# Kernel optimization log

Measured on AMD Instinct MI355X. Metric: run time of the kernel, lower is better.

Reference implementation:

```python
import jax, jax.numpy as jnp
import numpy as np

B, N, H, HEADS, L = 8, 64, 512, 8, 4
VOCAB, NBOND, CLS = 128, 8, 2
SP = H // HEADS
SCALE = float(np.sqrt(H))  # module divides by sqrt(hidden_dim), not sqrt(sp_dim)


def _ln(x):
    # fresh nn.LayerNorm each call -> gamma=1, beta=0
    m = jnp.mean(x, -1, keepdims=True)
    v = jnp.mean((x - m) ** 2, -1, keepdims=True)
    return (x - m) / jnp.sqrt(v + 1e-5)


def _split(x):  # [B,N,H] -> [B,h,N,sp]
    return x.reshape(B, N, HEADS, SP).transpose(0, 2, 1, 3)


def setup_inputs() -> dict:
    key = jax.random.key(0)
    ks = jax.random.split(key, 16)
    s = 0.05
    return {
        "input_batch": jax.random.randint(ks[0], (B, N), 0, VOCAB),
        "adj_m": jax.random.randint(ks[1], (B, N, N), 0, NBOND),
        "atom_emb": jax.random.normal(ks[2], (VOCAB, H), jnp.float32) * s,
        "bond_emb": jax.random.normal(ks[3], (NBOND, H), jnp.float32) * s,
        "Wq": jax.random.normal(ks[4], (L, H, H), jnp.float32) * s,
        "Wk": jax.random.normal(ks[5], (L, H, H), jnp.float32) * s,
        "Wv": jax.random.normal(ks[6], (L, H, H), jnp.float32) * s,
        "Wew": jax.random.normal(ks[7], (L, H, H), jnp.float32) * s,
        "Wstack": jax.random.normal(ks[8], (L, H, H), jnp.float32) * s,
        "Wf1": jax.random.normal(ks[9], (L, H, 4 * H), jnp.float32) * s,
        "Wf2": jax.random.normal(ks[10], (L, 4 * H, H), jnp.float32) * s,
        "Wout": jax.random.normal(ks[11], (H, H), jnp.float32) * s,
        "Wpred": jax.random.normal(ks[12], (H, CLS), jnp.float32) * s,
        "bpred": jnp.zeros((CLS,), jnp.float32),
    }


def _forward(input_batch, adj_m, atom_emb, bond_emb, Wq, Wk, Wv, Wew,
             Wstack, Wf1, Wf2, Wout, Wpred, bpred):
    x = atom_emb[input_batch]        # [B,N,H] atom embeddings
    bond = bond_emb[adj_m]           # [B,N,N,H] bond embeddings
    neg = jnp.where(adj_m > 0, 0.0, -jnp.inf)[:, None, :, :]  # [B,1,N,N]
    for l in range(L):
        xn = _ln(x)
        q = _split(xn @ Wq[l])
        k = _split(xn @ Wk[l])
        v = _split(xn @ Wv[l])
        ew = bond @ Wew[l]           # [B,N,N,H]
        w = ew.reshape(B, N, N, HEADS, SP).transpose(0, 3, 1, 2, 4)  # [B,h,N,N,sp]
        # bond_influence==1: sim_ij = q_i . (k_j + w_ij)
        logits = jnp.einsum('bhid,bhjd->bhij', q, k) \
               + jnp.einsum('bhid,bhijd->bhij', q, w)
        attn = jax.nn.softmax(logits / SCALE + neg, axis=-1)
        o = jnp.einsum('bhij,bhjd->bhid', attn, v)
        o = o.transpose(0, 2, 1, 3).reshape(B, N, H) @ Wstack[l]
        attn_resid = o + xn
        ff = jax.nn.relu(_ln(attn_resid) @ Wf1[l]) @ Wf2[l]
        x = ff + attn_resid          # transformer_output
        # edge attention update: softmax over {w.w, w.x_i, w.x_j}
        ew_s = jnp.sum(ew * ew, -1)                      # [B,N,N]
        a0 = jnp.einsum('bijh,bih->bij', ew, x)
        a1 = jnp.einsum('bijh,bjh->bij', ew, x)
        wgt = jax.nn.softmax(jnp.stack([ew_s, a0, a1], -1) / SCALE, -1)  # [B,N,N,3]
        bond = (wgt[..., 0:1] * ew
                + wgt[..., 1:2] * x[:, :, None, :]
                + wgt[..., 2:3] * x[:, None, :, :])      # new edge state
    cls = jnp.tanh(x[:, 0, :] @ Wout)
    return jax.nn.softmax(cls @ Wpred + bpred, axis=-1)


def reference(input_batch, adj_m, atom_emb, bond_emb, Wq, Wk, Wv, Wew,
              Wstack, Wf1, Wf2, Wout, Wpred, bpred):
    return _forward(input_batch, adj_m, atom_emb, bond_emb, Wq, Wk, Wv, Wew,
                    Wstack, Wf1, Wf2, Wout, Wpred, bpred)
```

## Files before the change

kernel.cpp:

```cpp
#include <hip/hip_runtime.h>
#include <hip/hip_bf16.h>

typedef __hip_bfloat16 bf16;

#define B_     8
#define N_     64
#define H_     512
#define HEADS_ 8
#define SP_    64
#define L_     4
static constexpr float INV_SCALE = 0.044194173824159216f;

typedef __attribute__((ext_vector_type(8))) short short8;
typedef __attribute__((ext_vector_type(4))) float f32x4;

__device__ __forceinline__ void unpack8(uint4 u, float* f) {
    f[0] = __uint_as_float(u.x << 16); f[1] = __uint_as_float(u.x & 0xffff0000u);
    f[2] = __uint_as_float(u.y << 16); f[3] = __uint_as_float(u.y & 0xffff0000u);
    f[4] = __uint_as_float(u.z << 16); f[5] = __uint_as_float(u.z & 0xffff0000u);
    f[6] = __uint_as_float(u.w << 16); f[7] = __uint_as_float(u.w & 0xffff0000u);
}

__device__ __forceinline__ bf16 f2bf(float v) { return __float2bfloat16(v); }

__device__ __forceinline__ uint4 pack8bf(float4 a, float4 b) {
    __align__(16) bf16 t[8];
    t[0] = f2bf(a.x); t[1] = f2bf(a.y); t[2] = f2bf(a.z); t[3] = f2bf(a.w);
    t[4] = f2bf(b.x); t[5] = f2bf(b.y); t[6] = f2bf(b.z); t[7] = f2bf(b.w);
    return *(const uint4*)t;
}

#define RSTR 80

template <int EPI>
__device__ __forceinline__ void gemm64_body(char* lds,
        const bf16* __restrict__ A, const bf16* __restrict__ Bt,
        void* __restrict__ Cv, const float* __restrict__ R,
        int M, int N, int K, int bx, int by, int kbeg, int kend) {
    char* As = lds;
    char* Bs = lds + 2 * 64 * RSTR;
    const int tid = threadIdx.x;
    const int bm = bx * 64, bn = by * 64;
    const int w = tid >> 6, lane = tid & 63;
    const int wr = (w >> 1) * 32, wc = (w & 1) * 32;
    const int m0 = lane & 15, q4 = lane >> 4;

    f32x4 acc[2][2] = {};

    const int rA = tid >> 3;
    const int cA = tid & 7;
    const int ksP = cA >> 2;
    const int cB = (cA & 3) * 16;
    const int cE = cA * 8;

    for (int k0 = kbeg; k0 < kend; k0 += 64) {
        uint4 a0 = *(const uint4*)(A  + (size_t)(bm + rA) * K + k0 + cE);
        uint4 a1 = *(const uint4*)(A  + (size_t)(bm + rA + 32) * K + k0 + cE);
        uint4 b0 = *(const uint4*)(Bt + (size_t)(bn + rA) * K + k0 + cE);
        uint4 b1 = *(const uint4*)(Bt + (size_t)(bn + rA + 32) * K + k0 + cE);
        __syncthreads();
        *(uint4*)(As + ksP * (64 * RSTR) + rA * RSTR + cB) = a0;
        *(uint4*)(As + ksP * (64 * RSTR) + (rA + 32) * RSTR + cB) = a1;
        *(uint4*)(Bs + ksP * (64 * RSTR) + rA * RSTR + cB) = b0;
        *(uint4*)(Bs + ksP * (64 * RSTR) + (rA + 32) * RSTR + cB) = b1;
        __syncthreads();
        short8 af[2][2], bfr[2][2];
        #pragma unroll
        for (int ks = 0; ks < 2; ++ks)
            #pragma unroll
            for (int t = 0; t < 2; ++t) {
                af[ks][t]  = *(const short8*)(As + ks * (64 * RSTR) + (wr + t * 16 + m0) * RSTR + q4 * 16);
                bfr[ks][t] = *(const short8*)(Bs + ks * (64 * RSTR) + (wc + t * 16 + m0) * RSTR + q4 * 16);
            }
        #pragma unroll
        for (int ks = 0; ks < 2; ++ks)
            #pragma unroll
            for (int mt = 0; mt < 2; ++mt)
                #pragma unroll
                for (int nt = 0; nt < 2; ++nt)
                    acc[mt][nt] = __builtin_amdgcn_mfma_f32_16x16x32_bf16(
                        af[ks][mt], bfr[ks][nt], acc[mt][nt], 0, 0, 0);
    }

    if (EPI <= 1) {
        float* C = (float*)Cv;
        #pragma unroll
        for (int mt = 0; mt < 2; ++mt)
            #pragma unroll
            for (int i = 0; i < 4; ++i) {
                int row = bm + wr + mt * 16 + q4 * 4 + i;
                #pragma unroll
                for (int nt = 0; nt < 2; ++nt) {
                    int col = bn + wc + nt * 16 + m0;
                    float v = acc[mt][nt][i];
                    if (EPI == 1) v += R[(size_t)row * N + col];
                    C[(size_t)row * N + col] = v;
                }
            }
    } else {
        bf16* C = (bf16*)Cv;
        #pragma unroll
        for (int mt = 0; mt < 2; ++mt)
            #pragma unroll
            for (int i = 0; i < 4; ++i) {
                int row = bm + wr + mt * 16 + q4 * 4 + i;
                #pragma unroll
                for (int nt = 0; nt < 2; ++nt) {
                    int col = bn + wc + nt * 16 + m0;
                    float v = acc[mt][nt][i];
                    if (EPI == 2) v = fmaxf(v, 0.0f);
                    C[(size_t)row * N + col] = __float2bfloat16(v);
                }
            }
    }
}

template <int EPI, bool SPLIT>
__launch_bounds__(256)
__global__ void mfma_gemm_s(const bf16* __restrict__ A, const bf16* __restrict__ Bt,
                            void* __restrict__ Cv, const float* __restrict__ R,
                            int M, int N, int K) {
    __shared__ __align__(16) char lds[4 * 64 * RSTR];
    int kbeg = 0, kend = K;
    const bf16* B2 = Bt;
    void* C2 = Cv;
    if (SPLIT) {
        int ks = K / gridDim.z;
        kbeg = blockIdx.z * ks;
        kend = kbeg + ks;
        C2 = (void*)((float*)Cv + (size_t)blockIdx.z * M * N);
        gemm64_body<0>(lds, A, B2, C2, nullptr, M, N, K, blockIdx.x, blockIdx.y, kbeg, kend);
    } else {
        B2 = Bt + (size_t)blockIdx.z * N * K;
        if (EPI <= 1) C2 = (void*)((float*)Cv + (size_t)blockIdx.z * M * N);
        gemm64_body<EPI>(lds, A, B2, C2, R, M, N, K, blockIdx.x, blockIdx.y, kbeg, kend);
    }
}

__launch_bounds__(256)
__global__ void basis1_qkv_kernel(const bf16* __restrict__ x_bf, const bf16* __restrict__ E0,
                                  const bf16* __restrict__ ewt1,
                                  bf16* __restrict__ xw1, bf16* __restrict__ e0w1,
                                  const bf16* __restrict__ xn_bf, const bf16* __restrict__ qkvt_l,
                                  float* __restrict__ qkv) {
    __shared__ __align__(16) char lds[4 * 64 * RSTR];
    int bx = blockIdx.x, by = blockIdx.y;
    if (bx < 8)
        gemm64_body<3>(lds, x_bf, ewt1, xw1, nullptr, 512, 512, 512, bx, by, 0, 512);
    else if (bx == 8)
        gemm64_body<3>(lds, E0, ewt1, e0w1, nullptr, 64, 512, 512, 0, by, 0, 512);
    else {
        int tq = bx - 9;
        int z = tq >> 3, mb = tq & 7;
        gemm64_body<0>(lds, xn_bf, qkvt_l + (size_t)z * 262144,
                       qkv + (size_t)z * 262144, nullptr, 512, 512, 512, mb, by, 0, 512);
    }
}

__launch_bounds__(256)
__global__ void basis2_qkv_kernel(const bf16* __restrict__ xw1, const bf16* __restrict__ x_bf,
                                  const bf16* __restrict__ e0w1, const bf16* __restrict__ ewt2,
                                  bf16* __restrict__ xw12, bf16* __restrict__ x2w2,
                                  bf16* __restrict__ e0w12,
                                  const bf16* __restrict__ xn_bf, const bf16* __restrict__ qkvt_l,
                                  float* __restrict__ qkv) {
    __shared__ __align__(16) char lds[4 * 64 * RSTR];
    int bx = blockIdx.x, by = blockIdx.y;
    if (bx < 8)
        gemm64_body<3>(lds, xw1, ewt2, xw12, nullptr, 512, 512, 512, bx, by, 0, 512);
    else if (bx < 16)
        gemm64_body<3>(lds, x_bf, ewt2, x2w2, nullptr, 512, 512, 512, bx - 8, by, 0, 512);
    else if (bx == 16)
        gemm64_body<3>(lds, e0w1, ewt2, e0w12, nullptr, 64, 512, 512, 0, by, 0, 512);
    else {
        int tq = bx - 17;
        int z = tq >> 3, mb = tq & 7;
        gemm64_body<0>(lds, xn_bf, qkvt_l + (size_t)z * 262144,
                       qkv + (size_t)z * 262144, nullptr, 512, 512, 512, mb, by, 0, 512);
    }
}

__launch_bounds__(256)
__global__ void ptable_kernel(const float* __restrict__ q,
                              const bf16* __restrict__ B0, const bf16* __restrict__ B1,
                              const bf16* __restrict__ B2,
                              float* __restrict__ P0, float* __restrict__ P1,
                              float* __restrict__ P2) {
    __shared__ __align__(16) char lds[4 * 64 * RSTR];
    char* As = lds;
    char* Bs = lds + 2 * 64 * RSTR;
    const int b = blockIdx.x, h = blockIdx.y, z = blockIdx.z;
    const int nz = gridDim.z;
    const bf16* Bt = (z == 0) ? B0 : (z == 1 ? B1 : B2);
    float* P = (z == 0) ? P0 : (z == 1 ? P1 : P2);
    const bool shr = (z == nz - 1);
    const int tid = threadIdx.x;
    const int w = tid >> 6, lane = tid & 63;
    const int wr = (w >> 1) * 32, wc = (w & 1) * 32;
    const int m0 = lane & 15, q4 = lane >> 4;
    const int rA = tid >> 3;
    const int cA = tid & 7;
    const int ksP = cA >> 2;
    const int cB = (cA & 3) * 16;
    const int cE = cA * 8;

    const float* Aq = q + (size_t)(b * 64) * 512 + h * 64;
    const bf16*  Bb = Bt + (shr ? (size_t)0 : (size_t)b * 64 * 512) + h * 64;

    float4 fa0 = *(const float4*)(Aq + (size_t)rA * 512 + cE);
    float4 fa1 = *(const float4*)(Aq + (size_t)rA * 512 + cE + 4);
    float4 fb0 = *(const float4*)(Aq + (size_t)(rA + 32) * 512 + cE);
    float4 fb1 = *(const float4*)(Aq + (size_t)(rA + 32) * 512 + cE + 4);
    uint4 bv0 = *(const uint4*)(Bb + (size_t)rA * 512 + cE);
    uint4 bv1 = *(const uint4*)(Bb + (size_t)(rA + 32) * 512 + cE);
    uint4 av0 = pack8bf(fa0, fa1);
    uint4 av1 = pack8bf(fb0, fb1);
    *(uint4*)(As + ksP * (64 * RSTR) + rA * RSTR + cB) = av0;
    *(uint4*)(As + ksP * (64 * RSTR) + (rA + 32) * RSTR + cB) = av1;
    *(uint4*)(Bs + ksP * (64 * RSTR) + rA * RSTR + cB) = bv0;
    *(uint4*)(Bs + ksP * (64 * RSTR) + (rA + 32) * RSTR + cB) = bv1;
    __syncthreads();

    f32x4 acc[2][2] = {};
    short8 af[2][2], bfr[2][2];
    #pragma unroll
    for (int ks = 0; ks < 2; ++ks)
        #pragma unroll
        for (int t = 0; t < 2; ++t) {
            af[ks][t]  = *(const short8*)(As + ks * (64 * RSTR) + (wr + t * 16 + m0) * RSTR + q4 * 16);
            bfr[ks][t] = *(const short8*)(Bs + ks * (64 * RSTR) + (wc + t * 16 + m0) * RSTR + q4 * 16);
        }
    #pragma unroll
    for (int ks = 0; ks < 2; ++ks)
        #pragma unroll
        for (int mt = 0; mt < 2; ++mt)
            #pragma unroll
            for (int nt = 0; nt < 2; ++nt)
                acc[mt][nt] = __builtin_amdgcn_mfma_f32_16x16x32_bf16(
                    af[ks][mt], bfr[ks][nt], acc[mt][nt], 0, 0, 0);

    #pragma unroll
    for (int mt = 0; mt < 2; ++mt)
        #pragma unroll
        for (int i = 0; i < 4; ++i) {
            int row = wr + mt * 16 + q4 * 4 + i;
            #pragma unroll
            for (int nt = 0; nt < 2; ++nt) {
                int col = wc + nt * 16 + m0;
                P[(((size_t)b * 8 + h) * 64 + row) * 64 + col] = acc[mt][nt][i];
            }
        }
}

__launch_bounds__(256)
__global__ void gram1_kernel(const bf16* __restrict__ xw1, const bf16* __restrict__ e0w1,
                             const bf16* __restrict__ xb, float* __restrict__ gbuf) {
    __shared__ __align__(16) char lds[4 * 64 * RSTR];
    int b = blockIdx.x, z = blockIdx.y;
    size_t ob = (size_t)b * 32768;
    const bf16 *A, *Bt;
    switch (z) {
        case 0: A = xw1 + ob; Bt = xw1 + ob; break;
        case 1: A = e0w1;     Bt = xw1 + ob; break;
        case 2: A = xw1 + ob; Bt = xb + ob;  break;
        case 3: A = e0w1;     Bt = xb + ob;  break;
        default: A = e0w1;    Bt = e0w1;     break;
    }
    float* C = gbuf + (size_t)z * 32768 + (size_t)b * 4096;
    gemm64_body<0>(lds, A, Bt, C, nullptr, 64, 64, 512, 0, 0, 0, 512);
}

__launch_bounds__(256)
__global__ void gram2_kernel(const bf16* __restrict__ xw12, const bf16* __restrict__ x2w2,
                             const bf16* __restrict__ e0w12, const bf16* __restrict__ xb,
                             float* __restrict__ gbuf) {
    __shared__ __align__(16) char lds[4 * 64 * RSTR];
    int b = blockIdx.x, z = blockIdx.y;
    size_t ob = (size_t)b * 32768;
    const bf16 *A, *Bt;
    switch (z) {
        case 0: A = xw12 + ob; Bt = xw12 + ob; break;
        case 1: A = xw12 + ob; Bt = x2w2 + ob; break;
        case 2: A = x2w2 + ob; Bt = x2w2 + ob; break;
        case 3: A = e0w12;     Bt = xw12 + ob; break;
        case 4: A = e0w12;     Bt = x2w2 + ob; break;
        case 5: A = e0w12;     Bt = e0w12;     break;
        case 6: A = xw12 + ob; Bt = xb + ob;   break;
        case 7: A = x2w2 + ob; Bt = xb + ob;   break;
        default: A = e0w12;    Bt = xb + ob;   break;
    }
    float* C = gbuf + (size_t)z * 32768 + (size_t)b * 4096;
    gemm64_body<0>(lds, A, Bt, C, nullptr, 64, 64, 512, 0, 0, 0, 512);
}

__global__ void coeff_assemble1(const int* __restrict__ adj,
        const float* __restrict__ c0a, const float* __restrict__ c1a, const float* __restrict__ c2a,
        const float* __restrict__ gbuf,
        float* __restrict__ w0o, float* __restrict__ w1o, float* __restrict__ w2o) {
    int bi = blockIdx.x;
    int b = bi >> 6, i = bi & 63;
    int j = threadIdx.x;
    int p = bi * 64 + j;
    int t = adj[p];
    const float* TXX = gbuf + 0 * 32768 + (size_t)b * 4096;
    const float* TEX = gbuf + 1 * 32768 + (size_t)b * 4096;
    const float* TXx = gbuf + 2 * 32768 + (size_t)b * 4096;
    const float* TEx = gbuf + 3 * 32768 + (size_t)b * 4096;
    const float* TEE = gbuf + 4 * 32768 + (size_t)b * 4096;
    float c0 = c0a[p], c1 = c1a[p], c2 = c2a[p];
    float s1 = c0 * TEx[t * 64 + i] + c1 * TXx[i * 64 + i] + c2 * TXx[j * 64 + i];
    float s2 = c0 * TEx[t * 64 + j] + c1 * TXx[i * 64 + j] + c2 * TXx[j * 64 + j];
    float s0 = c0 * c0 * TEE[t * 64 + t] + c1 * c1 * TXX[i * 64 + i] + c2 * c2 * TXX[j * 64 + j]
             + 2.f * c0 * c1 * TEX[t * 64 + i] + 2.f * c0 * c2 * TEX[t * 64 + j]
             + 2.f * c1 * c2 * TXX[i * 64 + j];
    float t0 = s0 * INV_SCALE, t1 = s1 * INV_SCALE, t2 = s2 * INV_SCALE;
    float m = fmaxf(t0, fmaxf(t1, t2));
    float e0 = expf(t0 - m), e1 = expf(t1 - m), e2 = expf(t2 - m);
    float inv = 1.0f / (e0 + e1 + e2);
    w0o[p] = e0 * inv;
    w1o[p] = e1 * inv;
    w2o[p] = e2 * inv;
}

__global__ void coeff_assemble2(const int* __restrict__ adj,
        const float* __restrict__ c0a, const float* __restrict__ c1a, const float* __restrict__ c2a,
        const float* __restrict__ c0b, const float* __restrict__ c1b, const float* __restrict__ c2b,
        const float* __restrict__ gbuf,
        float* __restrict__ w0o, float* __restrict__ w1o, float* __restrict__ w2o) {
    int bi = blockIdx.x;
    int b = bi >> 6, i = bi & 63;
    int j = threadIdx.x;
    int p = bi * 64 + j;
    int t = adj[p];
    const float* TXX = gbuf + 0 * 32768 + (size_t)b * 4096;
    const float* TXY = gbuf + 1 * 32768 + (size_t)b * 4096;
    const float* TYY = gbuf + 2 * 32768 + (size_t)b * 4096;
    const float* TEX = gbuf + 3 * 32768 + (size_t)b * 4096;
    const float* TEY = gbuf + 4 * 32768 + (size_t)b * 4096;
    const float* TEE = gbuf + 5 * 32768 + (size_t)b * 4096;
    const float* TXx = gbuf + 6 * 32768 + (size_t)b * 4096;
    const float* TYx = gbuf + 7 * 32768 + (size_t)b * 4096;
    const float* TEx = gbuf + 8 * 32768 + (size_t)b * 4096;
    float a0 = c0b[p];
    float AE = a0 * c0a[p], Aa = a0 * c1a[p], Ab = a0 * c2a[p];
    float Ac = c1b[p], Ad = c2b[p];
    float s1 = AE * TEx[t * 64 + i] + Aa * TXx[i * 64 + i] + Ab * TXx[j * 64 + i]
             + Ac * TYx[i * 64 + i] + Ad * TYx[j * 64 + i];
    float s2 = AE * TEx[t * 64 + j] + Aa * TXx[i * 64 + j] + Ab * TXx[j * 64 + j]
             + Ac * TYx[i * 64 + j] + Ad * TYx[j * 64 + j];
    float s0 = AE * AE * TEE[t * 64 + t] + Aa * Aa * TXX[i * 64 + i] + Ab * Ab * TXX[j * 64 + j]
             + Ac * Ac * TYY[i * 64 + i] + Ad * Ad * TYY[j * 64 + j]
             + 2.f * AE * Aa * TEX[t * 64 + i] + 2.f * AE * Ab * TEX[t * 64 + j]
             + 2.f * AE * Ac * TEY[t * 64 + i] + 2.f * AE * Ad * TEY[t * 64 + j]
             + 2.f * Aa * Ab * TXX[i * 64 + j]
             + 2.f * Aa * Ac * TXY[i * 64 + i] + 2.f * Aa * Ad * TXY[i * 64 + j]
             + 2.f * Ab * Ac * TXY[j * 64 + i] + 2.f * Ab * Ad * TXY[j * 64 + j]
             + 2.f * Ac * Ad * TYY[i * 64 + j];
    float t0 = s0 * INV_SCALE, t1 = s1 * INV_SCALE, t2 = s2 * INV_SCALE;
    float m = fmaxf(t0, fmaxf(t1, t2));
    float e0 = expf(t0 - m), e1 = expf(t1 - m), e2 = expf(t2 - m);
    float inv = 1.0f / (e0 + e1 + e2);
    w0o[p] = e0 * inv;
    w1o[p] = e1 * inv;
    w2o[p] = e2 * inv;
}

__launch_bounds__(256)
__global__ void u_gemm(const float* __restrict__ q, const bf16* __restrict__ wc3,
                       bf16* __restrict__ ubf) {
    __shared__ __align__(16) char lds[4 * 64 * RSTR];
    char* As = lds;
    char* Bs = lds + 2 * 64 * RSTR;
    const int h = blockIdx.x, mb = blockIdx.y, nb = blockIdx.z;
    const int tid = threadIdx.x;
    const int w = tid >> 6, lane = tid & 63;
    const int wr = (w >> 1) * 32, wc = (w & 1) * 32;
    const int m0 = lane & 15, q4 = lane >> 4;
    const int rA = tid >> 3;
    const int cA = tid & 7;
    const int ksP = cA >> 2;
    const int cB = (cA & 3) * 16;
    const int cE = cA * 8;

    const float* Aq = q + (size_t)(mb * 64) * 512 + h * 64;
    const bf16*  Bt = wc3 + (size_t)(nb * 64) * 512 + h * 64;

    float4 fa0 = *(const float4*)(Aq + (size_t)rA * 512 + cE);
    float4 fa1 = *(const float4*)(Aq + (size_t)rA * 512 + cE + 4);
    float4 fb0 = *(const float4*)(Aq + (size_t)(rA + 32) * 512 + cE);
    float4 fb1 = *(const float4*)(Aq + (size_t)(rA + 32) * 512 + cE + 4);
    uint4 b0 = *(const uint4*)(Bt + (size_t)rA * 512 + cE);
    uint4 b1 = *(const uint4*)(Bt + (size_t)(rA + 32) * 512 + cE);
    uint4 a0 = pack8bf(fa0, fa1);
    uint4 a1 = pack8bf(fb0, fb1);
    *(uint4*)(As + ksP * (64 * RSTR) + rA * RSTR + cB) = a0;
    *(uint4*)(As + ksP * (64 * RSTR) + (rA + 32) * RSTR + cB) = a1;
    *(uint4*)(Bs + ksP * (64 * RSTR) + rA * RSTR + cB) = b0;
    *(uint4*)(Bs + ksP * (64 * RSTR) + (rA + 32) * RSTR + cB) = b1;
    __syncthreads();

    f32x4 acc[2][2] = {};
    short8 af[2][2], bfr[2][2];
    #pragma unroll
    for (int ks = 0; ks < 2; ++ks)
        #pragma unroll
        for (int t = 0; t < 2; ++t) {
            af[ks][t]  = *(const short8*)(As + ks * (64 * RSTR) + (wr + t * 16 + m0) * RSTR + q4 * 16);
            bfr[ks][t] = *(const short8*)(Bs + ks * (64 * RSTR) + (wc + t * 16 + m0) * RSTR + q4 * 16);
        }
    #pragma unroll
    for (int ks = 0; ks < 2; ++ks)
        #pragma unroll
        for (int mt = 0; mt < 2; ++mt)
            #pragma unroll
            for (int nt = 0; nt < 2; ++nt)
                acc[mt][nt] = __builtin_amdgcn_mfma_f32_16x16x32_bf16(
                    af[ks][mt], bfr[ks][nt], acc[mt][nt], 0, 0, 0);

    #pragma unroll
    for (int mt = 0; mt < 2; ++mt)
        #pragma unroll
        for (int i = 0; i < 4; ++i) {
            int row = mb * 64 + wr + mt * 16 + q4 * 4 + i;
            #pragma unroll
            for (int nt = 0; nt < 2; ++nt) {
                int col = nb * 64 + wc + nt * 16 + m0;
                ubf[(size_t)row * 4096 + h * 512 + col] = f2bf(acc[mt][nt][i]);
            }
        }
}

__global__ void cast_w3(const float* __restrict__ in, bf16* __restrict__ out) {
    int gid = blockIdx.x * 256 + threadIdx.x;
    const float4* p = (const float4*)(in + (size_t)gid * 8);
    float4 a = p[0], b = p[1];
    *(uint4*)(out + (size_t)gid * 8) = pack8bf(a, b);
}

__launch_bounds__(256)
__global__ void mbuf_gemm(const bf16* __restrict__ ubf, const bf16* __restrict__ xw12,
                          const bf16* __restrict__ x2w2, const bf16* __restrict__ x_bf,
                          const bf16* __restrict__ e0w12,
                          float* __restrict__ MX, float* __restrict__ MY,
                          float* __restrict__ MZ, float* __restrict__ DE) {
    __shared__ __align__(16) char lds[4 * 64 * RSTR];
    int b = blockIdx.x, mt = blockIdx.y, z = blockIdx.z;
    const bf16* A = ubf + (size_t)b * 512 * 512;
    const bf16* Bt;
    float* C;
    if (z == 0)      { Bt = xw12 + (size_t)b * 64 * 512; C = MX + (size_t)b * 512 * 64; }
    else if (z == 1) { Bt = x2w2 + (size_t)b * 64 * 512; C = MY + (size_t)b * 512 * 64; }
    else if (z == 2) { Bt = x_bf + (size_t)b * 64 * 512; C = MZ + (size_t)b * 512 * 64; }
    else             { Bt = e0w12;                        C = DE + (size_t)b * 512 * 64; }
    gemm64_body<0>(lds, A, Bt, C, nullptr, 512, 64, 512, mt, 0, 0, 512);
}

__global__ void s2_assemble(const int* __restrict__ adj,
        const float* __restrict__ c0a, const float* __restrict__ c1a, const float* __restrict__ c2a,
        const float* __restrict__ c0b, const float* __restrict__ c1b, const float* __restrict__ c2b,
        const float* __restrict__ v0c, const float* __restrict__ v1c, const float* __restrict__ v2c,
        const float* __restrict__ MX, const float* __restrict__ MY,
        const float* __restrict__ MZ, const float* __restrict__ DE,
        float* __restrict__ s2) {
    int bi = blockIdx.x;
    int b = bi >> 6, i = bi & 63;
    int j = threadIdx.x, h = threadIdx.y;
    int p = bi * 64 + j;
    float v0 = v0c[p];
    float q0 = v0 * c0b[p];
    float AE = q0 * c0a[p], Aa = q0 * c1a[p], Ab = q0 * c2a[p];
    float Ac = v0 * c1b[p], Ad = v0 * c2b[p];
    float Ae = v1c[p], Af = v2c[p];
    size_t rb = ((size_t)b * 512 + i * 8 + h) * 64;
    float s = AE * DE[rb + adj[p]]
            + Aa * MX[rb + i] + Ac * MY[rb + i] + Ae * MZ[rb + i]
            + Ab * MX[rb + j] + Ad * MY[rb + j] + Af * MZ[rb + j];
    s2[(((size_t)b * 8 + h) * 64 + i) * 64 + j] = s;
}

__global__ void embed_ln_kernel(const int* __restrict__ ids,
                                const float* __restrict__ emb,
                                float* __restrict__ xn, bf16* __restrict__ xn_bf) {
    int row = blockIdx.x;
    int tid = threadIdx.x;
    const float* r = emb + (size_t)ids[row] * H_;
    float x0 = r[tid], x1 = r[tid + 256];
    float s = x0 + x1, sq = x0 * x0 + x1 * x1;
    #pragma unroll
    for (int off = 32; off; off >>= 1) {
        s  += __shfl_xor(s,  off);
        sq += __shfl_xor(sq, off);
    }
    __shared__ float ls[4], lq[4];
    int w = tid >> 6;
    if ((tid & 63) == 0) { ls[w] = s; lq[w] = sq; }
    __syncthreads();
    float S = ls[0] + ls[1] + ls[2] + ls[3];
    float Q = lq[0] + lq[1] + lq[2] + lq[3];
    float mean = S * (1.0f / H_);
    float var  = Q * (1.0f / H_) - mean * mean;
    float inv  = rsqrtf(var + 1e-5f);
    float y0 = (x0 - mean) * inv, y1 = (x1 - mean) * inv;
    xn[(size_t)row * H_ + tid]       = y0;
    xn[(size_t)row * H_ + tid + 256] = y1;
    xn_bf[(size_t)row * H_ + tid]       = f2bf(y0);
    xn_bf[(size_t)row * H_ + tid + 256] = f2bf(y1);
}

__global__ void ew0_precompute(const float* __restrict__ bond_emb,
                               const bf16* __restrict__ ewt0, bf16* __restrict__ E0) {
    int t = blockIdx.x, cb = blockIdx.y, lane = threadIdx.x;
    int c = cb * 64 + lane;
    if (t >= 8) { E0[t * 512 + c] = f2bf(0.0f); return; }
    __shared__ float be[512];
    for (int h = lane; h < 512; h += 64) be[h] = bond_emb[t * 512 + h];
    __syncthreads();
    const bf16* wr = ewt0 + (size_t)c * 512;
    float acc = 0.f;
    for (int h8 = 0; h8 < 64; ++h8) {
        uint4 u = *(const uint4*)(wr + h8 * 8);
        float wf[8];
        unpack8(u, wf);
        const float* b = &be[h8 * 8];
        acc += b[0]*wf[0] + b[1]*wf[1] + b[2]*wf[2] + b[3]*wf[3]
             + b[4]*wf[4] + b[5]*wf[5] + b[6]*wf[6] + b[7]*wf[7];
    }
    E0[t * 512 + c] = f2bf(acc);
}

__global__ void transpose_sq(const float* __restrict__ Wq, const float* __restrict__ Wk,
                             const float* __restrict__ Wv, const float* __restrict__ Wew,
                             const float* __restrict__ Wst,
                             bf16* __restrict__ qkvt, bf16* __restrict__ ewt,
                             bf16* __restrict__ stackt) {
    const size_t KN = (size_t)H_ * H_;
    int z = blockIdx.z;
    const float* W; bf16* Wt;
    if (z < 12) {
        int s = z >> 2, l = z & 3;
        W  = (s == 0 ? Wq : s == 1 ? Wk : Wv) + (size_t)l * KN;
        Wt = qkvt + (size_t)l * 3 * KN + (size_t)s * KN;
    } else if (z < 16) {
        int l = z - 12;
        W = Wew + (size_t)l * KN; Wt = ewt + (size_t)l * KN;
    } else {
        int l = z - 16;
        W = Wst + (size_t)l * KN; Wt = stackt + (size_t)l * KN;
    }
    __shared__ float t[32][33];
    int k0 = blockIdx.x * 32, n0 = blockIdx.y * 32;
    int tx = threadIdx.x, ty = threadIdx.y;
    #pragma unroll
    for (int r = ty; r < 32; r += 8)
        t[r][tx] = W[(size_t)(k0 + r) * H_ + n0 + tx];
    __syncthreads();
    #pragma unroll
    for (int r = ty; r < 32; r += 8)
        Wt[(size_t)(n0 + r) * H_ + k0 + tx] = f2bf(t[tx][r]);
}

__global__ void transpose_rect(const float* __restrict__ Wf1, const float* __restrict__ Wf2,
                               bf16* __restrict__ f1t, bf16* __restrict__ f2t) {
    const size_t KN4 = (size_t)4 * H_ * H_;
    int z = blockIdx.z;
    const float* W; bf16* Wt; int K, N;
    if (z < 4) {
        if (blockIdx.x >= 16) return;
        W = Wf1 + (size_t)z * KN4; Wt = f1t + (size_t)z * KN4; K = 512; N = 2048;
    } else {
        if (blockIdx.y >= 16) return;
        W = Wf2 + (size_t)(z - 4) * KN4; Wt = f2t + (size_t)(z - 4) * KN4; K = 2048; N = 512;
    }
    __shared__ float t[32][33];
    int k0 = blockIdx.x * 32, n0 = blockIdx.y * 32;
    int tx = threadIdx.x, ty = threadIdx.y;
    #pragma unroll
    for (int r = ty; r < 32; r += 8)
        t[r][tx] = W[(size_t)(k0 + r) * N + n0 + tx];
    __syncthreads();
    #pragma unroll
    for (int r = ty; r < 32; r += 8)
        Wt[(size_t)(n0 + r) * K + k0 + tx] = f2bf(t[tx][r]);
}

__global__ void reduce_stack_ln(const float* __restrict__ part, const float* __restrict__ base,
                                float* __restrict__ resid, bf16* __restrict__ ffin_bf) {
    const int MN = 512 * H_;
    int row = blockIdx.x;
    int tid = threadIdx.x;
    size_t b0 = (size_t)row * H_;
    float v0 = base[b0 + tid], v1 = base[b0 + tid + 256];
    #pragma unroll
    for (int s = 0; s < 4; ++s) {
        v0 += part[(size_t)s * MN + b0 + tid];
        v1 += part[(size_t)s * MN + b0 + tid + 256];
    }
    resid[b0 + tid] = v0;
    resid[b0 + tid + 256] = v1;
    float s = v0 + v1, sq = v0 * v0 + v1 * v1;
    #pragma unroll
    for (int off = 32; off; off >>= 1) {
        s  += __shfl_xor(s,  off);
        sq += __shfl_xor(sq, off);
    }
    __shared__ float ls[4], lq[4];
    int w = tid >> 6;
    if ((tid & 63) == 0) { ls[w] = s; lq[w] = sq; }
    __syncthreads();
    float S = ls[0] + ls[1] + ls[2] + ls[3];
    float Q = lq[0] + lq[1] + lq[2] + lq[3];
    float mean = S * (1.0f / H_);
    float var  = Q * (1.0f / H_) - mean * mean;
    float inv  = rsqrtf(var + 1e-5f);
    ffin_bf[b0 + tid]       = f2bf((v0 - mean) * inv);
    ffin_bf[b0 + tid + 256] = f2bf((v1 - mean) * inv);
}

template <bool DO_LN>
__global__ void reduce_ln_kernel(const float* __restrict__ part, const float* __restrict__ resid,
                                 float* __restrict__ x, bf16* __restrict__ x_bf,
                                 float* __restrict__ xn, bf16* __restrict__ xn_bf) {
    const int MN = 512 * H_;
    int row = blockIdx.x;
    int tid = threadIdx.x;
    size_t base = (size_t)row * H_;
    float v0 = resid[base + tid], v1 = resid[base + tid + 256];
    #pragma unroll
    for (int s = 0; s < 4; ++s) {
        v0 += part[(size_t)s * MN + base + tid];
        v1 += part[(size_t)s * MN + base + tid + 256];
    }
    x[base + tid] = v0;
    x[base + tid + 256] = v1;
    x_bf[base + tid]       = f2bf(v0);
    x_bf[base + tid + 256] = f2bf(v1);
    if (DO_LN) {
        float s = v0 + v1, sq = v0 * v0 + v1 * v1;
        #pragma unroll
        for (int off = 32; off; off >>= 1) {
            s  += __shfl_xor(s,  off);
            sq += __shfl_xor(sq, off);
        }
        __shared__ float ls[4], lq[4];
        int w = tid >> 6;
        if ((tid & 63) == 0) { ls[w] = s; lq[w] = sq; }
        __syncthreads();
        float S = ls[0] + ls[1] + ls[2] + ls[3];
        float Q = lq[0] + lq[1] + lq[2] + lq[3];
        float mean = S * (1.0f / H_);
        float var  = Q * (1.0f / H_) - mean * mean;
        float inv  = rsqrtf(var + 1e-5f);
        float y0 = (v0 - mean) * inv, y1 = (v1 - mean) * inv;
        xn[base + tid]       = y0;
        xn[base + tid + 256] = y1;
        xn_bf[base + tid]       = f2bf(y0);
        xn_bf[base + tid + 256] = f2bf(y1);
    }
}

template <bool GATHER>
__global__ void attn_kernel(const float* __restrict__ qkv, const bf16* __restrict__ ew,
                            const int* __restrict__ adj, bf16* __restrict__ o) {
    const float* q = qkv;
    const float* k = qkv + (size_t)512 * H_;
    const float* v = qkv + (size_t)1024 * H_;
    int bi = blockIdx.x;
    int b  = bi >> 6;
    int ty = threadIdx.y;
    int h  = blockIdx.y * 4 + ty;
    int lane = threadIdx.x;
    __shared__ float qs[4][64], as[4][64];
    qs[ty][lane] = q[(size_t)bi * H_ + h * 64 + lane];
    __syncthreads();

    int j = lane;
    int pair = bi * 64 + j;
    int aj = adj[pair];
    const float4* k4 = (const float4*)(k + (size_t)(b * 64 + j) * H_ + h * 64);
    const uint4*  w4 = (const uint4*)((GATHER ? ew + (size_t)aj * H_
                                              : ew + (size_t)pair * H_) + h * 64);
    float acc = 0.f;
    #pragma unroll
    for (int t = 0; t < 8; ++t) {
        uint4 wu = w4[t];
        float4 ka = k4[2 * t], kb = k4[2 * t + 1];
        float wf[8];
        unpack8(wu, wf);
        const float* qq = &qs[ty][t * 8];
        acc += qq[0] * (ka.x + wf[0]) + qq[1] * (ka.y + wf[1])
             + qq[2] * (ka.z + wf[2]) + qq[3] * (ka.w + wf[3])
             + qq[4] * (kb.x + wf[4]) + qq[5] * (kb.y + wf[5])
             + qq[6] * (kb.z + wf[6]) + qq[7] * (kb.w + wf[7]);
    }
    float logit = acc * INV_SCALE;
    if (aj <= 0) logit = -INFINITY;

    float m = logit;
    #pragma unroll
    for (int off = 32; off; off >>= 1) m = fmaxf(m, __shfl_xor(m, off));
    float p = expf(logit - m);
    float s = p;
    #pragma unroll
    for (int off = 32; off; off >>= 1) s += __shfl_xor(s, off);
    as[ty][lane] = p / s;
    __syncthreads();

    const float* vbase = v + (size_t)(b * 64) * H_ + h * 64;
    float oacc = 0.f;
    int d = lane;
    #pragma unroll 8
    for (int jj = 0; jj < 64; ++jj)
        oacc += as[ty][jj] * vbase[(size_t)jj * H_ + d];
    o[(size_t)bi * H_ + h * 64 + d] = __float2bfloat16(oacc);
}

template <int MODE>
__global__ void attn13_kernel(const float* __restrict__ qkv, const int* __restrict__ adj,
        const float* __restrict__ c0a, const float* __restrict__ c1a, const float* __restrict__ c2a,
        const float* __restrict__ c0b, const float* __restrict__ c1b, const float* __restrict__ c2b,
        const float* __restrict__ PX, const float* __restrict__ PY, const float* __restrict__ PE,
        bf16* __restrict__ o) {
    const float* q = qkv;
    const float* k = qkv + (size_t)512 * H_;
    const float* v = qkv + (size_t)1024 * H_;
    int bi = blockIdx.x;
    int b  = bi >> 6, i = bi & 63;
    int ty = threadIdx.y;
    int h  = blockIdx.y * 4 + ty;
    int lane = threadIdx.x;
    __shared__ float qs[4][64], as[4][64];
    qs[ty][lane] = q[(size_t)bi * H_ + h * 64 + lane];
    __syncthreads();

    int j = lane;
    int p = bi * 64 + j;
    int t = adj[p];
    size_t pb = (((size_t)b * 8 + h) * 64 + i) * 64;
    float acc;
    if (MODE == 1) {
        acc = c0a[p] * PE[pb + t] + c1a[p] * PX[pb + i] + c2a[p] * PX[pb + j];
    } else {
        float a0 = c0b[p];
        float AE = a0 * c0a[p], Aa = a0 * c1a[p], Ab = a0 * c2a[p];
        float Ac = c1b[p], Ad = c2b[p];
        acc = AE * PE[pb + t] + Aa * PX[pb + i] + Ab * PX[pb + j]
            + Ac * PY[pb + i] + Ad * PY[pb + j];
    }
    const float4* k4 = (const float4*)(k + (size_t)(b * 64 + j) * H_ + h * 64);
    #pragma unroll
    for (int tt = 0; tt < 8; ++tt) {
        float4 ka = k4[2 * tt], kb = k4[2 * tt + 1];
        const float* qq = &qs[ty][tt * 8];
        acc += qq[0] * ka.x + qq[1] * ka.y + qq[2] * ka.z + qq[3] * ka.w
             + qq[4] * kb.x + qq[5] * kb.y + qq[6] * kb.z + qq[7] * kb.w;
    }
    float logit = acc * INV_SCALE;
    if (t <= 0) logit = -INFINITY;

    float m = logit;
    #pragma unroll
    for (int off = 32; off; off >>= 1) m = fmaxf(m, __shfl_xor(m, off));
    float pe = expf(logit - m);
    float s = pe;
    #pragma unroll
    for (int off = 32; off; off >>= 1) s += __shfl_xor(s, off);
    as[ty][lane] = pe / s;
    __syncthreads();

    const float* vbase = v + (size_t)(b * 64) * H_ + h * 64;
    float oacc = 0.f;
    int d = lane;
    #pragma unroll 8
    for (int jj = 0; jj < 64; ++jj)
        oacc += as[ty][jj] * vbase[(size_t)jj * H_ + d];
    o[(size_t)bi * H_ + h * 64 + d] = __float2bfloat16(oacc);
}

__global__ void attn3_kernel(const float* __restrict__ qkv, const float* __restrict__ s2,
                             const int* __restrict__ adj, bf16* __restrict__ o) {
    const float* q = qkv;
    const float* k = qkv + (size_t)512 * H_;
    const float* v = qkv + (size_t)1024 * H_;
    int bi = blockIdx.x;
    int b  = bi >> 6, i = bi & 63;
    int ty = threadIdx.y;
    int h  = blockIdx.y * 4 + ty;
    int lane = threadIdx.x;
    __shared__ float qs[4][64], as[4][64];
    qs[ty][lane] = q[(size_t)bi * H_ + h * 64 + lane];
    __syncthreads();

    int j = lane;
    const float4* k4 = (const float4*)(k + (size_t)(b * 64 + j) * H_ + h * 64);
    float acc = s2[(((size_t)b * 8 + h) * 64 + i) * 64 + j];
    #pragma unroll
    for (int t = 0; t < 8; ++t) {
        float4 ka = k4[2 * t], kb = k4[2 * t + 1];
        const float* qq = &qs[ty][t * 8];
        acc += qq[0] * ka.x + qq[1] * ka.y + qq[2] * ka.z + qq[3] * ka.w
             + qq[4] * kb.x + qq[5] * kb.y + qq[6] * kb.z + qq[7] * kb.w;
    }
    float logit = acc * INV_SCALE;
    if (adj[(size_t)bi * 64 + j] <= 0) logit = -INFINITY;

    float m = logit;
    #pragma unroll
    for (int off = 32; off; off >>= 1) m = fmaxf(m, __shfl_xor(m, off));
    float p = expf(logit - m);
    float s = p;
    #pragma unroll
    for (int off = 32; off; off >>= 1) s += __shfl_xor(s, off);
    as[ty][lane] = p / s;
    __syncthreads();

    const float* vbase = v + (size_t)(b * 64) * H_ + h * 64;
    float oacc = 0.f;
    int d = lane;
    #pragma unroll 8
    for (int jj = 0; jj < 64; ++jj)
        oacc += as[ty][jj] * vbase[(size_t)jj * H_ + d];
    o[(size_t)bi * H_ + h * 64 + d] = __float2bfloat16(oacc);
}

template <bool GATHER>
__global__ void edge_coeff_kernel(const bf16* __restrict__ ewsrc, const int* __restrict__ adj,
                                  const float* __restrict__ x,
                                  float* __restrict__ w0o, float* __restrict__ w1o,
                                  float* __restrict__ w2o) {
    int pair = blockIdx.x * 4 + threadIdx.y;
    int b = pair >> 12;
    int i = (pair >> 6) & 63;
    int j = pair & 63;
    int lane = threadIdx.x;
    const uint4*  e4  = (const uint4*)(GATHER ? ewsrc + (size_t)adj[pair] * H_
                                              : ewsrc + (size_t)pair * H_);
    const float4* xi4 = (const float4*)(x + (size_t)(b * 64 + i) * H_);
    const float4* xj4 = (const float4*)(x + (size_t)(b * 64 + j) * H_);
    uint4  eu = e4[lane];
    float4 a0 = xi4[lane * 2], a1 = xi4[lane * 2 + 1];
    float4 c0 = xj4[lane * 2], c1 = xj4[lane * 2 + 1];
    float ef[8], af[8], cf[8];
    unpack8(eu, ef);
    af[0] = a0.x; af[1] = a0.y; af[2] = a0.z; af[3] = a0.w;
    af[4] = a1.x; af[5] = a1.y; af[6] = a1.z; af[7] = a1.w;
    cf[0] = c0.x; cf[1] = c0.y; cf[2] = c0.z; cf[3] = c0.w;
    cf[4] = c1.x; cf[5] = c1.y; cf[6] = c1.z; cf[7] = c1.w;
    float s0 = 0.f, s1 = 0.f, s2 = 0.f;
    #pragma unroll
    for (int t = 0; t < 8; ++t) {
        s0 += ef[t] * ef[t]; s1 += ef[t] * af[t]; s2 += ef[t] * cf[t];
    }
    #pragma unroll
    for (int off = 32; off; off >>= 1) {
        s0 += __shfl_xor(s0, off);
        s1 += __shfl_xor(s1, off);
        s2 += __shfl_xor(s2, off);
    }
    float t0 = s0 * INV_SCALE, t1 = s1 * INV_SCALE, t2 = s2 * INV_SCALE;
    float m = fmaxf(t0, fmaxf(t1, t2));
    float e0 = expf(t0 - m), e1 = expf(t1 - m), e2 = expf(t2 - m);
    float inv = 1.0f / (e0 + e1 + e2);
    if (lane == 0) {
        w0o[pair] = e0 * inv;
        w1o[pair] = e1 * inv;
        w2o[pair] = e2 * inv;
    }
}

__global__ void cls_part_kernel(const float* __restrict__ x, const float* __restrict__ Wout,
                                float* __restrict__ clspart) {
    int b  = blockIdx.x;
    int cb = blockIdx.y;
    int ks = blockIdx.z;
    int tid = threadIdx.x;
    int c  = cb * 64 + (tid & 63);
    int kk = tid >> 6;
    const float* xr = x + (size_t)(b * 64) * H_;
    int h0 = ks * 128 + kk * 32;
    float acc = 0.f;
    #pragma unroll
    for (int h = 0; h < 32; ++h)
        acc += xr[h0 + h] * Wout[(size_t)(h0 + h) * H_ + c];
    __shared__ float red[4][64];
    red[kk][tid & 63] = acc;
    __syncthreads();
    if (tid < 64) {
        float v = red[0][tid] + red[1][tid] + red[2][tid] + red[3][tid];
        clspart[((size_t)ks * 8 + b) * H_ + cb * 64 + tid] = v;
    }
}

__global__ void cls_pred2_kernel(const float* __restrict__ clspart,
                                 const float* __restrict__ Wpred,
                                 const float* __restrict__ bpred,
                                 float* __restrict__ out) {
    int b = blockIdx.x;
    int tid = threadIdx.x;
    __shared__ float red0[4], red1[4];
    float a0 = 0.f, a1 = 0.f;
    #pragma unroll
    for (int t = 0; t < 2; ++t) {
        int c = tid + t * 256;
        float v = clspart[((size_t)0 * 8 + b) * H_ + c]
                + clspart[((size_t)1 * 8 + b) * H_ + c]
                + clspart[((size_t)2 * 8 + b) * H_ + c]
                + clspart[((size_t)3 * 8 + b) * H_ + c];
        float tv = tanhf(v);
        a0 += tv * Wpred[c * 2 + 0];
        a1 += tv * Wpred[c * 2 + 1];
    }
    #pragma unroll
    for (int off = 32; off; off >>= 1) {
        a0 += __shfl_xor(a0, off);
        a1 += __shfl_xor(a1, off);
    }
    int w = tid >> 6;
    if ((tid & 63) == 0) { red0[w] = a0; red1[w] = a1; }
    __syncthreads();
    if (tid == 0) {
        float s0 = red0[0] + red0[1] + red0[2] + red0[3] + bpred[0];
        float s1 = red1[0] + red1[1] + red1[2] + red1[3] + bpred[1];
        float m = fmaxf(s0, s1);
        float e0 = expf(s0 - m), e1 = expf(s1 - m);
        float inv = 1.0f / (e0 + e1);
        out[b * 2 + 0] = e0 * inv;
        out[b * 2 + 1] = e1 * inv;
    }
}

extern "C" void kernel_launch(void* const* d_in, const int* in_sizes, int n_in,
                              void* d_out, int out_size, void* d_ws, size_t ws_size,
                              hipStream_t stream) {
    const int*   ids      = (const int*)d_in[0];
    const int*   adj      = (const int*)d_in[1];
    const float* atom_emb = (const float*)d_in[2];
    const float* bond_emb = (const float*)d_in[3];
    const float* Wq     = (const float*)d_in[4];
    const float* Wk     = (const float*)d_in[5];
    const float* Wv     = (const float*)d_in[6];
    const float* Wew    = (const float*)d_in[7];
    const float* Wstack = (const float*)d_in[8];
    const float* Wf1    = (const float*)d_in[9];
    const float* Wf2    = (const float*)d_in[10];
    const float* Wout   = (const float*)d_in[11];
    const float* Wpred  = (const float*)d_in[12];
    const float* bpred  = (const float*)d_in[13];

    char* ws = (char*)d_ws;
    size_t off = 0;
    auto alloc = [&](size_t bytes) {
        size_t o = off;
        off += (bytes + 255) & ~(size_t)255;
        return o;
    };
    const size_t ROWS  = (size_t)B_ * N_;
    const size_t PAIRS = (size_t)B_ * N_ * N_;
    const size_t KN    = (size_t)H_ * H_;

    float* x       = (float*)(ws + alloc(ROWS * H_ * 4));
    float* xn      = (float*)(ws + alloc(ROWS * H_ * 4));
    bf16*  xn_bf   = (bf16*) (ws + alloc(ROWS * H_ * 2));
    bf16*  x_bf    = (bf16*) (ws + alloc(ROWS * H_ * 2));
    float* qkv     = (float*)(ws + alloc(3 * ROWS * H_ * 4));
    bf16*  o_bf    = (bf16*) (ws + alloc(ROWS * H_ * 2));
    float* resid   = (float*)(ws + alloc(ROWS * H_ * 4));
    bf16*  ffin_bf = (bf16*) (ws + alloc(ROWS * H_ * 2));
    bf16*  ffh_bf  = (bf16*) (ws + alloc(ROWS * 4 * H_ * 2));
    float* part    = (float*)(ws + alloc(4 * ROWS * H_ * 4));
    float* clspart = (float*)(ws + alloc(4 * 8 * H_ * 4));
    bf16*  ubf     = (bf16*) (ws + alloc(ROWS * 8 * 512 * 2));
    float* s2buf   = (float*)(ws + alloc((size_t)B_ * 8 * 64 * 64 * 4));
    float* MX      = (float*)(ws + alloc((size_t)4096 * 64 * 4));
    float* MY      = (float*)(ws + alloc((size_t)4096 * 64 * 4));
    float* MZ      = (float*)(ws + alloc((size_t)4096 * 64 * 4));
    float* DE      = (float*)(ws + alloc((size_t)4096 * 64 * 4));
    float* PT0     = (float*)(ws + alloc((size_t)4096 * 64 * 4));
    float* PT1     = (float*)(ws + alloc((size_t)4096 * 64 * 4));
    float* PT2     = (float*)(ws + alloc((size_t)4096 * 64 * 4));
    float* gbuf    = (float*)(ws + alloc((size_t)9 * 8 * 4096 * 4));
    bf16*  wc3     = (bf16*) (ws + alloc(KN * 2));
    bf16*  E0      = (bf16*) (ws + alloc(64 * H_ * 2));
    bf16*  e0w1    = (bf16*) (ws + alloc(64 * H_ * 2));
    bf16*  e0w12   = (bf16*) (ws + alloc(64 * H_ * 2));
    bf16*  xw1     = (bf16*) (ws + alloc(KN * 2));
    bf16*  xw12    = (bf16*) (ws + alloc(KN * 2));
    bf16*  x2w2    = (bf16*) (ws + alloc(KN * 2));
    float* cw      = (float*)(ws + alloc(9 * PAIRS * 4));
    bf16*  qkvt    = (bf16*) (ws + alloc((size_t)L_ * 3 * KN * 2));
    bf16*  ewt     = (bf16*) (ws + alloc((size_t)L_ * KN * 2));
    bf16*  stackt  = (bf16*) (ws + alloc((size_t)L_ * KN * 2));
    bf16*  f1t     = (bf16*) (ws + alloc((size_t)L_ * 4 * KN * 2));
    bf16*  f2t     = (bf16*) (ws + alloc((size_t)L_ * 4 * KN * 2));
    (void)ws_size;

    float* cw0a = cw;
    float* cw1a = cw + PAIRS;
    float* cw2a = cw + 2 * PAIRS;
    float* cw0b = cw + 3 * PAIRS;
    float* cw1b = cw + 4 * PAIRS;
    float* cw2b = cw + 5 * PAIRS;
    float* cw0c = cw + 6 * PAIRS;
    float* cw1c = cw + 7 * PAIRS;
    float* cw2c = cw + 8 * PAIRS;

    embed_ln_kernel<<<512, 256, 0, stream>>>(ids, atom_emb, xn, xn_bf);

    dim3 tb(32, 8);
    transpose_sq<<<dim3(16, 16, 20), tb, 0, stream>>>(Wq, Wk, Wv, Wew, Wstack,
                                                      qkvt, ewt, stackt);
    transpose_rect<<<dim3(64, 64, 8), tb, 0, stream>>>(Wf1, Wf2, f1t, f2t);

    ew0_precompute<<<dim3(64, 8), 64, 0, stream>>>(bond_emb, ewt, E0);
    cast_w3<<<128, 256, 0, stream>>>(Wew + 3 * KN, wc3);

    for (int l = 0; l < L_; ++l) {
        if (l == 0) {
            mfma_gemm_s<0, false><<<dim3(8, 8, 3), 256, 0, stream>>>(
                xn_bf, qkvt, qkv, nullptr, 512, 512, 512);
            attn_kernel<true><<<dim3(512, 2), dim3(64, 4), 0, stream>>>(qkv, E0, adj, o_bf);
        } else if (l == 1) {
            basis1_qkv_kernel<<<dim3(33, 8), 256, 0, stream>>>(
                x_bf, E0, ewt + KN, xw1, e0w1, xn_bf, qkvt + (size_t)3 * KN, qkv);
            ptable_kernel<<<dim3(8, 8, 2), 256, 0, stream>>>(
                qkv, xw1, e0w1, nullptr, PT0, PT1, nullptr);
            attn13_kernel<1><<<dim3(512, 2), dim3(64, 4), 0, stream>>>(
                qkv, adj, cw0a, cw1a, cw2a, nullptr, nullptr, nullptr,
                PT0, nullptr, PT1, o_bf);
        } else if (l == 2) {
            basis2_qkv_kernel<<<dim3(41, 8), 256, 0, stream>>>(
                xw1, x_bf, e0w1, ewt + 2 * KN, xw12, x2w2, e0w12,
                xn_bf, qkvt + (size_t)6 * KN, qkv);
            ptable_kernel<<<dim3(8, 8, 3), 256, 0, stream>>>(
                qkv, xw12, x2w2, e0w12, PT0, PT1, PT2);
            attn13_kernel<2><<<dim3(512, 2), dim3(64, 4), 0, stream>>>(
                qkv, adj, cw0a, cw1a, cw2a, cw0b, cw1b, cw2b,
                PT0, PT1, PT2, o_bf);
        } else {
            mfma_gemm_s<0, false><<<dim3(8, 8, 3), 256, 0, stream>>>(
                xn_bf, qkvt + (size_t)9 * KN, qkv, nullptr, 512, 512, 512);
            u_gemm<<<dim3(8, 8, 8), 256, 0, stream>>>(qkv, wc3, ubf);
            mbuf_gemm<<<dim3(8, 8, 4), 256, 0, stream>>>(ubf, xw12, x2w2, x_bf, e0w12,
                                                         MX, MY, MZ, DE);
            s2_assemble<<<512, dim3(64, 8), 0, stream>>>(adj,
                cw0a, cw1a, cw2a, cw0b, cw1b, cw2b, cw0c, cw1c, cw2c,
                MX, MY, MZ, DE, s2buf);
            attn3_kernel<<<dim3(512, 2), dim3(64, 4), 0, stream>>>(qkv, s2buf, adj, o_bf);
        }

        mfma_gemm_s<0, true><<<dim3(8, 8, 4), 256, 0, stream>>>(
            o_bf, stackt + (size_t)l * KN, part, nullptr, 512, 512, 512);
        reduce_stack_ln<<<512, 256, 0, stream>>>(part, xn, resid, ffin_bf);
        mfma_gemm_s<2, false><<<dim3(8, 32), 256, 0, stream>>>(
            ffin_bf, f1t + (size_t)l * 4 * KN, ffh_bf, nullptr, 512, 2048, 512);
        mfma_gemm_s<0, true><<<dim3(8, 8, 4), 256, 0, stream>>>(
            ffh_bf, f2t + (size_t)l * 4 * KN, part, nullptr, 512, 512, 2048);
        if (l < L_ - 1)
            reduce_ln_kernel<true><<<512, 256, 0, stream>>>(part, resid, x, x_bf, xn, xn_bf);
        else
            reduce_ln_kernel<false><<<512, 256, 0, stream>>>(part, resid, x, x_bf, xn, xn_bf);

        if (l == 0) {
            edge_coeff_kernel<true><<<8192, dim3(64, 4), 0, stream>>>(
                E0, adj, x, cw0a, cw1a, cw2a);
        } else if (l == 1) {
            gram1_kernel<<<dim3(8, 5), 256, 0, stream>>>(xw1, e0w1, x_bf, gbuf);
            coeff_assemble1<<<512, 64, 0, stream>>>(adj, cw0a, cw1a, cw2a, gbuf,
                                                    cw0b, cw1b, cw2b);
        } else if (l == 2) {
            gram2_kernel<<<dim3(8, 9), 256, 0, stream>>>(xw12, x2w2, e0w12, x_bf, gbuf);
            coeff_assemble2<<<512, 64, 0, stream>>>(adj, cw0a, cw1a, cw2a,
                                                    cw0b, cw1b, cw2b, gbuf,
                                                    cw0c, cw1c, cw2c);
        }
    }

    cls_part_kernel<<<dim3(8, 8, 4), 256, 0, stream>>>(x, Wout, clspart);
    cls_pred2_kernel<<<8, 256, 0, stream>>>(clspart, Wpred, bpred, (float*)d_out);
}
```

Baseline: 393.5 us.

## Fuse setup, edge-coefficient, gram and assembly kernels into fewer launches

Merges the five setup kernels (embed+LN, weight transposes, E0 precompute, W3 cast) into one large setup kernel. It also folds each layer's edge-coefficient, gram and coefficient-assembly work into the next layer's basis/QKV, ptable and u-gemm kernels. The s2 assembly is fused into the layer-3 attention kernel, which removes the s2buf round trip. The aim is to cut kernel-launch count and small-grid latency across the dependency chain, at the cost of heterogeneous, branchy blocks and tighter cross-stage ordering.

```diff
diff --git a/kernel.cpp b/kernel.cpp
--- a/kernel.cpp
+++ b/kernel.cpp
@@ -137,63 +137,11 @@
     }
 }
 
-__launch_bounds__(256)
-__global__ void basis1_qkv_kernel(const bf16* __restrict__ x_bf, const bf16* __restrict__ E0,
-                                  const bf16* __restrict__ ewt1,
-                                  bf16* __restrict__ xw1, bf16* __restrict__ e0w1,
-                                  const bf16* __restrict__ xn_bf, const bf16* __restrict__ qkvt_l,
-                                  float* __restrict__ qkv) {
-    __shared__ __align__(16) char lds[4 * 64 * RSTR];
-    int bx = blockIdx.x, by = blockIdx.y;
-    if (bx < 8)
-        gemm64_body<3>(lds, x_bf, ewt1, xw1, nullptr, 512, 512, 512, bx, by, 0, 512);
-    else if (bx == 8)
-        gemm64_body<3>(lds, E0, ewt1, e0w1, nullptr, 64, 512, 512, 0, by, 0, 512);
-    else {
-        int tq = bx - 9;
-        int z = tq >> 3, mb = tq & 7;
-        gemm64_body<0>(lds, xn_bf, qkvt_l + (size_t)z * 262144,
-                       qkv + (size_t)z * 262144, nullptr, 512, 512, 512, mb, by, 0, 512);
-    }
-}
-
-__launch_bounds__(256)
-__global__ void basis2_qkv_kernel(const bf16* __restrict__ xw1, const bf16* __restrict__ x_bf,
-                                  const bf16* __restrict__ e0w1, const bf16* __restrict__ ewt2,
-                                  bf16* __restrict__ xw12, bf16* __restrict__ x2w2,
-                                  bf16* __restrict__ e0w12,
-                                  const bf16* __restrict__ xn_bf, const bf16* __restrict__ qkvt_l,
-                                  float* __restrict__ qkv) {
-    __shared__ __align__(16) char lds[4 * 64 * RSTR];
-    int bx = blockIdx.x, by = blockIdx.y;
-    if (bx < 8)
-        gemm64_body<3>(lds, xw1, ewt2, xw12, nullptr, 512, 512, 512, bx, by, 0, 512);
-    else if (bx < 16)
-        gemm64_body<3>(lds, x_bf, ewt2, x2w2, nullptr, 512, 512, 512, bx - 8, by, 0, 512);
-    else if (bx == 16)
-        gemm64_body<3>(lds, e0w1, ewt2, e0w12, nullptr, 64, 512, 512, 0, by, 0, 512);
-    else {
-        int tq = bx - 17;
-        int z = tq >> 3, mb = tq & 7;
-        gemm64_body<0>(lds, xn_bf, qkvt_l + (size_t)z * 262144,
-                       qkv + (size_t)z * 262144, nullptr, 512, 512, 512, mb, by, 0, 512);
-    }
-}
-
-__launch_bounds__(256)
-__global__ void ptable_kernel(const float* __restrict__ q,
-                              const bf16* __restrict__ B0, const bf16* __restrict__ B1,
-                              const bf16* __restrict__ B2,
-                              float* __restrict__ P0, float* __restrict__ P1,
-                              float* __restrict__ P2) {
-    __shared__ __align__(16) char lds[4 * 64 * RSTR];
+
+__device__ __forceinline__ void ptable_body(char* lds, const float* __restrict__ q,
+        const bf16* __restrict__ Bt, float* __restrict__ P, int b, int h, bool shr) {
     char* As = lds;
     char* Bs = lds + 2 * 64 * RSTR;
-    const int b = blockIdx.x, h = blockIdx.y, z = blockIdx.z;
-    const int nz = gridDim.z;
-    const bf16* Bt = (z == 0) ? B0 : (z == 1 ? B1 : B2);
-    float* P = (z == 0) ? P0 : (z == 1 ? P1 : P2);
-    const bool shr = (z == nz - 1);
     const int tid = threadIdx.x;
     const int w = tid >> 6, lane = tid & 63;
     const int wr = (w >> 1) * 32, wc = (w & 1) * 32;
@@ -252,55 +200,74 @@
         }
 }
 
-__launch_bounds__(256)
-__global__ void gram1_kernel(const bf16* __restrict__ xw1, const bf16* __restrict__ e0w1,
-                             const bf16* __restrict__ xb, float* __restrict__ gbuf) {
-    __shared__ __align__(16) char lds[4 * 64 * RSTR];
-    int b = blockIdx.x, z = blockIdx.y;
-    size_t ob = (size_t)b * 32768;
-    const bf16 *A, *Bt;
-    switch (z) {
-        case 0: A = xw1 + ob; Bt = xw1 + ob; break;
-        case 1: A = e0w1;     Bt = xw1 + ob; break;
-        case 2: A = xw1 + ob; Bt = xb + ob;  break;
-        case 3: A = e0w1;     Bt = xb + ob;  break;
-        default: A = e0w1;    Bt = e0w1;     break;
-    }
-    float* C = gbuf + (size_t)z * 32768 + (size_t)b * 4096;
-    gemm64_body<0>(lds, A, Bt, C, nullptr, 64, 64, 512, 0, 0, 0, 512);
-}
-
-__launch_bounds__(256)
-__global__ void gram2_kernel(const bf16* __restrict__ xw12, const bf16* __restrict__ x2w2,
-                             const bf16* __restrict__ e0w12, const bf16* __restrict__ xb,
-                             float* __restrict__ gbuf) {
-    __shared__ __align__(16) char lds[4 * 64 * RSTR];
-    int b = blockIdx.x, z = blockIdx.y;
-    size_t ob = (size_t)b * 32768;
-    const bf16 *A, *Bt;
-    switch (z) {
-        case 0: A = xw12 + ob; Bt = xw12 + ob; break;
-        case 1: A = xw12 + ob; Bt = x2w2 + ob; break;
-        case 2: A = x2w2 + ob; Bt = x2w2 + ob; break;
-        case 3: A = e0w12;     Bt = xw12 + ob; break;
-        case 4: A = e0w12;     Bt = x2w2 + ob; break;
-        case 5: A = e0w12;     Bt = e0w12;     break;
-        case 6: A = xw12 + ob; Bt = xb + ob;   break;
-        case 7: A = x2w2 + ob; Bt = xb + ob;   break;
-        default: A = e0w12;    Bt = xb + ob;   break;
-    }
-    float* C = gbuf + (size_t)z * 32768 + (size_t)b * 4096;
-    gemm64_body<0>(lds, A, Bt, C, nullptr, 64, 64, 512, 0, 0, 0, 512);
-}
-
-__global__ void coeff_assemble1(const int* __restrict__ adj,
+__device__ __forceinline__ void ugemm_body(char* lds, const float* __restrict__ q,
+        const bf16* __restrict__ wc3, bf16* __restrict__ ubf, int h, int mb, int nb) {
+    char* As = lds;
+    char* Bs = lds + 2 * 64 * RSTR;
+    const int tid = threadIdx.x;
+    const int w = tid >> 6, lane = tid & 63;
+    const int wr = (w >> 1) * 32, wc = (w & 1) * 32;
+    const int m0 = lane & 15, q4 = lane >> 4;
+    const int rA = tid >> 3;
+    const int cA = tid & 7;
+    const int ksP = cA >> 2;
+    const int cB = (cA & 3) * 16;
+    const int cE = cA * 8;
+
+    const float* Aq = q + (size_t)(mb * 64) * 512 + h * 64;
+    const bf16*  Bt = wc3 + (size_t)(nb * 64) * 512 + h * 64;
+
+    float4 fa0 = *(const float4*)(Aq + (size_t)rA * 512 + cE);
+    float4 fa1 = *(const float4*)(Aq + (size_t)rA * 512 + cE + 4);
+    float4 fb0 = *(const float4*)(Aq + (size_t)(rA + 32) * 512 + cE);
+    float4 fb1 = *(const float4*)(Aq + (size_t)(rA + 32) * 512 + cE + 4);
+    uint4 b0 = *(const uint4*)(Bt + (size_t)rA * 512 + cE);
+    uint4 b1 = *(const uint4*)(Bt + (size_t)(rA + 32) * 512 + cE);
+    uint4 a0 = pack8bf(fa0, fa1);
+    uint4 a1 = pack8bf(fb0, fb1);
+    *(uint4*)(As + ksP * (64 * RSTR) + rA * RSTR + cB) = a0;
+    *(uint4*)(As + ksP * (64 * RSTR) + (rA + 32) * RSTR + cB) = a1;
+    *(uint4*)(Bs + ksP * (64 * RSTR) + rA * RSTR + cB) = b0;
+    *(uint4*)(Bs + ksP * (64 * RSTR) + (rA + 32) * RSTR + cB) = b1;
+    __syncthreads();
+
+    f32x4 acc[2][2] = {};
+    short8 af[2][2], bfr[2][2];
+    #pragma unroll
+    for (int ks = 0; ks < 2; ++ks)
+        #pragma unroll
+        for (int t = 0; t < 2; ++t) {
+            af[ks][t]  = *(const short8*)(As + ks * (64 * RSTR) + (wr + t * 16 + m0) * RSTR + q4 * 16);
+            bfr[ks][t] = *(const short8*)(Bs + ks * (64 * RSTR) + (wc + t * 16 + m0) * RSTR + q4 * 16);
+        }
+    #pragma unroll
+    for (int ks = 0; ks < 2; ++ks)
+        #pragma unroll
+        for (int mt = 0; mt < 2; ++mt)
+            #pragma unroll
+            for (int nt = 0; nt < 2; ++nt)
+                acc[mt][nt] = __builtin_amdgcn_mfma_f32_16x16x32_bf16(
+                    af[ks][mt], bfr[ks][nt], acc[mt][nt], 0, 0, 0);
+
+    #pragma unroll
+    for (int mt = 0; mt < 2; ++mt)
+        #pragma unroll
+        for (int i = 0; i < 4; ++i) {
+            int row = mb * 64 + wr + mt * 16 + q4 * 4 + i;
+            #pragma unroll
+            for (int nt = 0; nt < 2; ++nt) {
+                int col = nb * 64 + wc + nt * 16 + m0;
+                ubf[(size_t)row * 4096 + h * 512 + col] = f2bf(acc[mt][nt][i]);
+            }
+        }
+}
+
+__device__ __forceinline__ void coeff1_body(const int* __restrict__ adj,
         const float* __restrict__ c0a, const float* __restrict__ c1a, const float* __restrict__ c2a,
-        const float* __restrict__ gbuf,
+        const float* __restrict__ gbuf, int row, int j,
         float* __restrict__ w0o, float* __restrict__ w1o, float* __restrict__ w2o) {
-    int bi = blockIdx.x;
-    int b = bi >> 6, i = bi & 63;
-    int j = threadIdx.x;
-    int p = bi * 64 + j;
+    int b = row >> 6, i = row & 63;
+    int p = row * 64 + j;
     int t = adj[p];
     const float* TXX = gbuf + 0 * 32768 + (size_t)b * 4096;
     const float* TEX = gbuf + 1 * 32768 + (size_t)b * 4096;
@@ -322,15 +289,13 @@
     w2o[p] = e2 * inv;
 }
 
-__global__ void coeff_assemble2(const int* __restrict__ adj,
+__device__ __forceinline__ void coeff2_body(const int* __restrict__ adj,
         const float* __restrict__ c0a, const float* __restrict__ c1a, const float* __restrict__ c2a,
         const float* __restrict__ c0b, const float* __restrict__ c1b, const float* __restrict__ c2b,
-        const float* __restrict__ gbuf,
+        const float* __restrict__ gbuf, int row, int j,
         float* __restrict__ w0o, float* __restrict__ w1o, float* __restrict__ w2o) {
-    int bi = blockIdx.x;
-    int b = bi >> 6, i = bi & 63;
-    int j = threadIdx.x;
-    int p = bi * 64 + j;
+    int b = row >> 6, i = row & 63;
+    int p = row * 64 + j;
     int t = adj[p];
     const float* TXX = gbuf + 0 * 32768 + (size_t)b * 4096;
     const float* TXY = gbuf + 1 * 32768 + (size_t)b * 4096;
@@ -366,75 +331,328 @@
 }
 
 __launch_bounds__(256)
-__global__ void u_gemm(const float* __restrict__ q, const bf16* __restrict__ wc3,
-                       bf16* __restrict__ ubf) {
+__global__ void setup_kernel(const int* __restrict__ ids, const float* __restrict__ atom_emb,
+                             const float* __restrict__ bond_emb,
+                             const float* __restrict__ Wq, const float* __restrict__ Wk,
+                             const float* __restrict__ Wv, const float* __restrict__ Wew,
+                             const float* __restrict__ Wst,
+                             const float* __restrict__ Wf1, const float* __restrict__ Wf2,
+                             float* __restrict__ xn, bf16* __restrict__ xn_bf,
+                             bf16* __restrict__ qkvt, bf16* __restrict__ ewt,
+                             bf16* __restrict__ stackt,
+                             bf16* __restrict__ f1t, bf16* __restrict__ f2t,
+                             bf16* __restrict__ E0, bf16* __restrict__ wc3) {
+    __shared__ float smem[32 * 33 + 8];
+    const size_t KN = (size_t)H_ * H_;
+    int bid = blockIdx.x;
+    int tid = threadIdx.x;
+
+    if (bid < 512) {
+        int row = bid;
+        const float* r = atom_emb + (size_t)ids[row] * H_;
+        float x0 = r[tid], x1 = r[tid + 256];
+        float s = x0 + x1, sq = x0 * x0 + x1 * x1;
+        #pragma unroll
+        for (int off = 32; off; off >>= 1) {
+            s  += __shfl_xor(s,  off);
+            sq += __shfl_xor(sq, off);
+        }
+        int w = tid >> 6;
+        if ((tid & 63) == 0) { smem[w] = s; smem[4 + w] = sq; }
+        __syncthreads();
+        float S = smem[0] + smem[1] + smem[2] + smem[3];
+        float Q = smem[4] + smem[5] + smem[6] + smem[7];
+        float mean = S * (1.0f / H_);
+        float var  = Q * (1.0f / H_) - mean * mean;
+        float inv  = rsqrtf(var + 1e-5f);
+        float y0 = (x0 - mean) * inv, y1 = (x1 - mean) * inv;
+        xn[(size_t)row * H_ + tid]       = y0;
+        xn[(size_t)row * H_ + tid + 256] = y1;
+        xn_bf[(size_t)row * H_ + tid]       = f2bf(y0);
+        xn_bf[(size_t)row * H_ + tid + 256] = f2bf(y1);
+    } else if (bid < 5632) {
+        int idx = bid - 512;
+        int z = idx >> 8;
+        int rem = idx & 255;
+        int byv = rem >> 4, bxv = rem & 15;
+        const float* W; bf16* Wt;
+        if (z < 12) {
+            int sss = z >> 2, l = z & 3;
+            W  = (sss == 0 ? Wq : sss == 1 ? Wk : Wv) + (size_t)l * KN;
+            Wt = qkvt + (size_t)l * 3 * KN + (size_t)sss * KN;
+        } else if (z < 16) {
+            int l = z - 12;
+            W = Wew + (size_t)l * KN; Wt = ewt + (size_t)l * KN;
+        } else {
+            int l = z - 16;
+            W = Wst + (size_t)l * KN; Wt = stackt + (size_t)l * KN;
+        }
+        float (*tt)[33] = (float(*)[33])smem;
+        int k0 = bxv * 32, n0 = byv * 32;
+        int tx = tid & 31, tyv = tid >> 5;
+        #pragma unroll
+        for (int rr = tyv; rr < 32; rr += 8)
+            tt[rr][tx] = W[(size_t)(k0 + rr) * H_ + n0 + tx];
+        __syncthreads();
+        #pragma unroll
+        for (int rr = tyv; rr < 32; rr += 8)
+            Wt[(size_t)(n0 + rr) * H_ + k0 + tx] = f2bf(tt[tx][rr]);
+    } else if (bid < 13824) {
+        int idx = bid - 5632;
+        int z = idx >> 10;
+        int idx2 = idx & 1023;
+        const size_t KN4 = (size_t)4 * H_ * H_;
+        const float* W; bf16* Wt; int K, N, kb, nb;
+        if (z < 4) {
+            W = Wf1 + (size_t)z * KN4; Wt = f1t + (size_t)z * KN4; K = 512; N = 2048;
+            kb = idx2 & 15; nb = idx2 >> 4;
+        } else {
+            W = Wf2 + (size_t)(z - 4) * KN4; Wt = f2t + (size_t)(z - 4) * KN4; K = 2048; N = 512;
+            kb = idx2 & 63; nb = idx2 >> 6;
+        }
+        float (*tt)[33] = (float(*)[33])smem;
+        int k0 = kb * 32, n0 = nb * 32;
+        int tx = tid & 31, tyv = tid >> 5;
+        #pragma unroll
+        for (int rr = tyv; rr < 32; rr += 8)
+            tt[rr][tx] = W[(size_t)(k0 + rr) * N + n0 + tx];
+        __syncthreads();
+        #pragma unroll
+        for (int rr = tyv; rr < 32; rr += 8)
+            Wt[(size_t)(n0 + rr) * K + k0 + tx] = f2bf(tt[tx][rr]);
+    } else if (bid < 13952) {
+        int idx = bid - 13824;
+        int t = idx >> 1;
+        int c = (idx & 1) * 256 + tid;
+        if (t >= 8) { E0[t * 512 + c] = f2bf(0.0f); return; }
+        float* be = smem;
+        be[tid]       = bond_emb[t * 512 + tid];
+        be[tid + 256] = bond_emb[t * 512 + tid + 256];
+        __syncthreads();
+        float acc = 0.f;
+        #pragma unroll 8
+        for (int h = 0; h < 512; ++h)
+            acc += be[h] * Wew[(size_t)h * 512 + c];
+        E0[t * 512 + c] = f2bf(acc);
+    } else {
+        int idx = bid - 13952;
+        int gid = idx * 256 + tid;
+        const float4* p = (const float4*)(Wew + 3 * KN + (size_t)gid * 8);
+        float4 a = p[0], b = p[1];
+        *(uint4*)(wc3 + (size_t)gid * 8) = pack8bf(a, b);
+    }
+}
+
+__launch_bounds__(256)
+__global__ void basis1_qkv_ec(const bf16* __restrict__ x_bf, const bf16* __restrict__ E0,
+                              const bf16* __restrict__ ewt1,
+                              bf16* __restrict__ xw1, bf16* __restrict__ e0w1,
+                              const bf16* __restrict__ xn_bf, const bf16* __restrict__ qkvt_l,
+                              float* __restrict__ qkv,
+                              const int* __restrict__ adj, const float* __restrict__ x,
+                              float* __restrict__ w0o, float* __restrict__ w1o,
+                              float* __restrict__ w2o) {
     __shared__ __align__(16) char lds[4 * 64 * RSTR];
-    char* As = lds;
-    char* Bs = lds + 2 * 64 * RSTR;
-    const int h = blockIdx.x, mb = blockIdx.y, nb = blockIdx.z;
-    const int tid = threadIdx.x;
-    const int w = tid >> 6, lane = tid & 63;
-    const int wr = (w >> 1) * 32, wc = (w & 1) * 32;
-    const int m0 = lane & 15, q4 = lane >> 4;
-    const int rA = tid >> 3;
-    const int cA = tid & 7;
-    const int ksP = cA >> 2;
-    const int cB = (cA & 3) * 16;
-    const int cE = cA * 8;
-
-    const float* Aq = q + (size_t)(mb * 64) * 512 + h * 64;
-    const bf16*  Bt = wc3 + (size_t)(nb * 64) * 512 + h * 64;
-
-    float4 fa0 = *(const float4*)(Aq + (size_t)rA * 512 + cE);
-    float4 fa1 = *(const float4*)(Aq + (size_t)rA * 512 + cE + 4);
-    float4 fb0 = *(const float4*)(Aq + (size_t)(rA + 32) * 512 + cE);
-    float4 fb1 = *(const float4*)(Aq + (size_t)(rA + 32) * 512 + cE + 4);
-    uint4 b0 = *(const uint4*)(Bt + (size_t)rA * 512 + cE);
-    uint4 b1 = *(const uint4*)(Bt + (size_t)(rA + 32) * 512 + cE);
-    uint4 a0 = pack8bf(fa0, fa1);
-    uint4 a1 = pack8bf(fb0, fb1);
-    *(uint4*)(As + ksP * (64 * RSTR) + rA * RSTR + cB) = a0;
-    *(uint4*)(As + ksP * (64 * RSTR) + (rA + 32) * RSTR + cB) = a1;
-    *(uint4*)(Bs + ksP * (64 * RSTR) + rA * RSTR + cB) = b0;
-    *(uint4*)(Bs + ksP * (64 * RSTR) + (rA + 32) * RSTR + cB) = b1;
-    __syncthreads();
-
-    f32x4 acc[2][2] = {};
-    short8 af[2][2], bfr[2][2];
-    #pragma unroll
-    for (int ks = 0; ks < 2; ++ks)
-        #pragma unroll
-        for (int t = 0; t < 2; ++t) {
-            af[ks][t]  = *(const short8*)(As + ks * (64 * RSTR) + (wr + t * 16 + m0) * RSTR + q4 * 16);
-            bfr[ks][t] = *(const short8*)(Bs + ks * (64 * RSTR) + (wc + t * 16 + m0) * RSTR + q4 * 16);
-        }
-    #pragma unroll
-    for (int ks = 0; ks < 2; ++ks)
-        #pragma unroll
-        for (int mt = 0; mt < 2; ++mt)
+    int bid = blockIdx.x;
+    if (bid < 264) {
+        int bx = bid >> 3, by = bid & 7;
+        if (bx < 8)
+            gemm64_body<3>(lds, x_bf, ewt1, xw1, nullptr, 512, 512, 512, bx, by, 0, 512);
+        else if (bx == 8)
+            gemm64_body<3>(lds, E0, ewt1, e0w1, nullptr, 64, 512, 512, 0, by, 0, 512);
+        else {
+            int tq = bx - 9;
+            int z = tq >> 3, mb = tq & 7;
+            gemm64_body<0>(lds, xn_bf, qkvt_l + (size_t)z * 262144,
+                           qkv + (size_t)z * 262144, nullptr, 512, 512, 512, mb, by, 0, 512);
+        }
+    } else {
+        int k = bid - 264;
+        int tid = threadIdx.x;
+        int lane = tid & 63, tyv = tid >> 6;
+        for (int pp = 0; pp < 4; ++pp) {
+            int pair = k * 16 + pp * 4 + tyv;
+            int b = pair >> 12;
+            int i = (pair >> 6) & 63;
+            int j = pair & 63;
+            const uint4*  e4  = (const uint4*)(E0 + (size_t)adj[pair] * H_);
+            const float4* xi4 = (const float4*)(x + (size_t)(b * 64 + i) * H_);
+            const float4* xj4 = (const float4*)(x + (size_t)(b * 64 + j) * H_);
+            uint4  eu = e4[lane];
+            float4 a0 = xi4[lane * 2], a1 = xi4[lane * 2 + 1];
+            float4 c0 = xj4[lane * 2], c1 = xj4[lane * 2 + 1];
+            float ef[8], af[8], cf[8];
+            unpack8(eu, ef);
+            af[0] = a0.x; af[1] = a0.y; af[2] = a0.z; af[3] = a0.w;
+            af[4] = a1.x; af[5] = a1.y; af[6] = a1.z; af[7] = a1.w;
+            cf[0] = c0.x; cf[1] = c0.y; cf[2] = c0.z; cf[3] = c0.w;
+            cf[4] = c1.x; cf[5] = c1.y; cf[6] = c1.z; cf[7] = c1.w;
+            float s0 = 0.f, s1 = 0.f, s2 = 0.f;
             #pragma unroll
-            for (int nt = 0; nt < 2; ++nt)
-                acc[mt][nt] = __builtin_amdgcn_mfma_f32_16x16x32_bf16(
-                    af[ks][mt], bfr[ks][nt], acc[mt][nt], 0, 0, 0);
-
-    #pragma unroll
-    for (int mt = 0; mt < 2; ++mt)
-        #pragma unroll
-        for (int i = 0; i < 4; ++i) {
-            int row = mb * 64 + wr + mt * 16 + q4 * 4 + i;
+            for (int t = 0; t < 8; ++t) {
+                s0 += ef[t] * ef[t]; s1 += ef[t] * af[t]; s2 += ef[t] * cf[t];
+            }
             #pragma unroll
-            for (int nt = 0; nt < 2; ++nt) {
-                int col = nb * 64 + wc + nt * 16 + m0;
-                ubf[(size_t)row * 4096 + h * 512 + col] = f2bf(acc[mt][nt][i]);
+            for (int off = 32; off; off >>= 1) {
+                s0 += __shfl_xor(s0, off);
+                s1 += __shfl_xor(s1, off);
+                s2 += __shfl_xor(s2, off);
             }
-        }
-}
-
-__global__ void cast_w3(const float* __restrict__ in, bf16* __restrict__ out) {
-    int gid = blockIdx.x * 256 + threadIdx.x;
-    const float4* p = (const float4*)(in + (size_t)gid * 8);
-    float4 a = p[0], b = p[1];
-    *(uint4*)(out + (size_t)gid * 8) = pack8bf(a, b);
+            float t0 = s0 * INV_SCALE, t1 = s1 * INV_SCALE, t2 = s2 * INV_SCALE;
+            float m = fmaxf(t0, fmaxf(t1, t2));
+            float e0 = expf(t0 - m), e1 = expf(t1 - m), e2 = expf(t2 - m);
+            float inv = 1.0f / (e0 + e1 + e2);
+            if (lane == 0) {
+                w0o[pair] = e0 * inv;
+                w1o[pair] = e1 * inv;
+                w2o[pair] = e2 * inv;
+            }
+        }
+    }
+}
+
+__launch_bounds__(256)
+__global__ void basis2_qkv_g1(const bf16* __restrict__ xw1, const bf16* __restrict__ x_bf,
+                              const bf16* __restrict__ e0w1, const bf16* __restrict__ ewt2,
+                              bf16* __restrict__ xw12, bf16* __restrict__ x2w2,
+                              bf16* __restrict__ e0w12,
+                              const bf16* __restrict__ xn_bf, const bf16* __restrict__ qkvt_l,
+                              float* __restrict__ qkv, float* __restrict__ gbuf) {
+    __shared__ __align__(16) char lds[4 * 64 * RSTR];
+    int bid = blockIdx.x;
+    if (bid < 328) {
+        int bx = bid >> 3, by = bid & 7;
+        if (bx < 8)
+            gemm64_body<3>(lds, xw1, ewt2, xw12, nullptr, 512, 512, 512, bx, by, 0, 512);
+        else if (bx < 16)
+            gemm64_body<3>(lds, x_bf, ewt2, x2w2, nullptr, 512, 512, 512, bx - 8, by, 0, 512);
+        else if (bx == 16)
+            gemm64_body<3>(lds, e0w1, ewt2, e0w12, nullptr, 64, 512, 512, 0, by, 0, 512);
+        else {
+            int tq = bx - 17;
+            int z = tq >> 3, mb = tq & 7;
+            gemm64_body<0>(lds, xn_bf, qkvt_l + (size_t)z * 262144,
+                           qkv + (size_t)z * 262144, nullptr, 512, 512, 512, mb, by, 0, 512);
+        }
+    } else {
+        int k = bid - 328;
+        int b = k & 7, z = k >> 3;
+        size_t ob = (size_t)b * 32768;
+        const bf16 *A, *Bt;
+        switch (z) {
+            case 0: A = xw1 + ob; Bt = xw1 + ob; break;
+            case 1: A = e0w1;     Bt = xw1 + ob; break;
+            case 2: A = xw1 + ob; Bt = x_bf + ob; break;
+            case 3: A = e0w1;     Bt = x_bf + ob; break;
+            default: A = e0w1;    Bt = e0w1;     break;
+        }
+        float* C = gbuf + (size_t)z * 32768 + (size_t)b * 4096;
+        gemm64_body<0>(lds, A, Bt, C, nullptr, 64, 64, 512, 0, 0, 0, 512);
+    }
+}
+
+__launch_bounds__(256)
+__global__ void ptable2c(const float* __restrict__ q,
+                         const bf16* __restrict__ B0, const bf16* __restrict__ B1,
+                         const bf16* __restrict__ B2,
+                         float* __restrict__ P0, float* __restrict__ P1,
+                         float* __restrict__ P2,
+                         const int* __restrict__ adj,
+                         const float* __restrict__ c0a, const float* __restrict__ c1a,
+                         const float* __restrict__ c2a, const float* __restrict__ gbuf,
+                         float* __restrict__ w0o, float* __restrict__ w1o,
+                         float* __restrict__ w2o) {
+    __shared__ __align__(16) char lds[4 * 64 * RSTR];
+    int bid = blockIdx.x;
+    if (bid < 192) {
+        int z = bid >> 6, rem = bid & 63;
+        int b = rem >> 3, h = rem & 7;
+        const bf16* Bt = (z == 0) ? B0 : (z == 1 ? B1 : B2);
+        float* P = (z == 0) ? P0 : (z == 1 ? P1 : P2);
+        ptable_body(lds, q, Bt, P, b, h, z == 2);
+    } else {
+        int k = bid - 192;
+        int tid = threadIdx.x;
+        int j = tid & 63;
+        #pragma unroll
+        for (int pass = 0; pass < 2; ++pass) {
+            int row = k * 8 + pass * 4 + (tid >> 6);
+            coeff1_body(adj, c0a, c1a, c2a, gbuf, row, j, w0o, w1o, w2o);
+        }
+    }
+}
+
+__launch_bounds__(256)
+__global__ void ptable_kernel(const float* __restrict__ q,
+                              const bf16* __restrict__ B0, const bf16* __restrict__ B1,
+                              float* __restrict__ P0, float* __restrict__ P1) {
+    __shared__ __align__(16) char lds[4 * 64 * RSTR];
+    const int b = blockIdx.x, h = blockIdx.y, z = blockIdx.z;
+    const bf16* Bt = (z == 0) ? B0 : B1;
+    float* P = (z == 0) ? P0 : P1;
+    ptable_body(lds, q, Bt, P, b, h, z == 1);
+}
+
+__launch_bounds__(256)
+__global__ void l3qkv_g2(const bf16* __restrict__ xn_bf, const bf16* __restrict__ qkvt_l,
+                         float* __restrict__ qkv,
+                         const bf16* __restrict__ xw12, const bf16* __restrict__ x2w2,
+                         const bf16* __restrict__ e0w12, const bf16* __restrict__ x_bf,
+                         float* __restrict__ gbuf) {
+    __shared__ __align__(16) char lds[4 * 64 * RSTR];
+    int bid = blockIdx.x;
+    if (bid < 192) {
+        int z = bid >> 6, rem = bid & 63;
+        int mb = rem >> 3, by = rem & 7;
+        gemm64_body<0>(lds, xn_bf, qkvt_l + (size_t)z * 262144,
+                       qkv + (size_t)z * 262144, nullptr, 512, 512, 512, mb, by, 0, 512);
+    } else {
+        int k = bid - 192;
+        int b = k & 7, z = k >> 3;
+        size_t ob = (size_t)b * 32768;
+        const bf16 *A, *Bt;
+        switch (z) {
+            case 0: A = xw12 + ob; Bt = xw12 + ob; break;
+            case 1: A = xw12 + ob; Bt = x2w2 + ob; break;
+            case 2: A = x2w2 + ob; Bt = x2w2 + ob; break;
+            case 3: A = e0w12;     Bt = xw12 + ob; break;
+            case 4: A = e0w12;     Bt = x2w2 + ob; break;
+            case 5: A = e0w12;     Bt = e0w12;     break;
+            case 6: A = xw12 + ob; Bt = x_bf + ob; break;
+            case 7: A = x2w2 + ob; Bt = x_bf + ob; break;
+            default: A = e0w12;    Bt = x_bf + ob; break;
+        }
+        float* C = gbuf + (size_t)z * 32768 + (size_t)b * 4096;
+        gemm64_body<0>(lds, A, Bt, C, nullptr, 64, 64, 512, 0, 0, 0, 512);
+    }
+}
+
+__launch_bounds__(256)
+__global__ void u_c2(const float* __restrict__ q, const bf16* __restrict__ wc3,
+                     bf16* __restrict__ ubf,
+                     const int* __restrict__ adj,
+                     const float* __restrict__ c0a, const float* __restrict__ c1a,
+                     const float* __restrict__ c2a,
+                     const float* __restrict__ c0b, const float* __restrict__ c1b,
+                     const float* __restrict__ c2b,
+                     const float* __restrict__ gbuf,
+                     float* __restrict__ w0o, float* __restrict__ w1o,
+                     float* __restrict__ w2o) {
+    __shared__ __align__(16) char lds[4 * 64 * RSTR];
+    int bid = blockIdx.x;
+    if (bid < 512) {
+        int h = bid >> 6, mb = (bid >> 3) & 7, nb = bid & 7;
+        ugemm_body(lds, q, wc3, ubf, h, mb, nb);
+    } else {
+        int k = bid - 512;
+        int tid = threadIdx.x;
+        int j = tid & 63;
+        #pragma unroll
+        for (int pass = 0; pass < 2; ++pass) {
+            int row = k * 8 + pass * 4 + (tid >> 6);
+            coeff2_body(adj, c0a, c1a, c2a, c0b, c1b, c2b, gbuf, row, j, w0o, w1o, w2o);
+        }
+    }
 }
 
 __launch_bounds__(256)
@@ -453,134 +671,6 @@
     else if (z == 2) { Bt = x_bf + (size_t)b * 64 * 512; C = MZ + (size_t)b * 512 * 64; }
     else             { Bt = e0w12;                        C = DE + (size_t)b * 512 * 64; }
     gemm64_body<0>(lds, A, Bt, C, nullptr, 512, 64, 512, mt, 0, 0, 512);
-}
-
-__global__ void s2_assemble(const int* __restrict__ adj,
-        const float* __restrict__ c0a, const float* __restrict__ c1a, const float* __restrict__ c2a,
-        const float* __restrict__ c0b, const float* __restrict__ c1b, const float* __restrict__ c2b,
-        const float* __restrict__ v0c, const float* __restrict__ v1c, const float* __restrict__ v2c,
-        const float* __restrict__ MX, const float* __restrict__ MY,
-        const float* __restrict__ MZ, const float* __restrict__ DE,
-        float* __restrict__ s2) {
-    int bi = blockIdx.x;
-    int b = bi >> 6, i = bi & 63;
-    int j = threadIdx.x, h = threadIdx.y;
-    int p = bi * 64 + j;
-    float v0 = v0c[p];
-    float q0 = v0 * c0b[p];
-    float AE = q0 * c0a[p], Aa = q0 * c1a[p], Ab = q0 * c2a[p];
-    float Ac = v0 * c1b[p], Ad = v0 * c2b[p];
-    float Ae = v1c[p], Af = v2c[p];
-    size_t rb = ((size_t)b * 512 + i * 8 + h) * 64;
-    float s = AE * DE[rb + adj[p]]
-            + Aa * MX[rb + i] + Ac * MY[rb + i] + Ae * MZ[rb + i]
-            + Ab * MX[rb + j] + Ad * MY[rb + j] + Af * MZ[rb + j];
-    s2[(((size_t)b * 8 + h) * 64 + i) * 64 + j] = s;
-}
-
-__global__ void embed_ln_kernel(const int* __restrict__ ids,
-                                const float* __restrict__ emb,
-                                float* __restrict__ xn, bf16* __restrict__ xn_bf) {
-    int row = blockIdx.x;
-    int tid = threadIdx.x;
-    const float* r = emb + (size_t)ids[row] * H_;
-    float x0 = r[tid], x1 = r[tid + 256];
-    float s = x0 + x1, sq = x0 * x0 + x1 * x1;
-    #pragma unroll
-    for (int off = 32; off; off >>= 1) {
-        s  += __shfl_xor(s,  off);
-        sq += __shfl_xor(sq, off);
-    }
-    __shared__ float ls[4], lq[4];
-    int w = tid >> 6;
-    if ((tid & 63) == 0) { ls[w] = s; lq[w] = sq; }
-    __syncthreads();
-    float S = ls[0] + ls[1] + ls[2] + ls[3];
-    float Q = lq[0] + lq[1] + lq[2] + lq[3];
-    float mean = S * (1.0f / H_);
-    float var  = Q * (1.0f / H_) - mean * mean;
-    float inv  = rsqrtf(var + 1e-5f);
-    float y0 = (x0 - mean) * inv, y1 = (x1 - mean) * inv;
-    xn[(size_t)row * H_ + tid]       = y0;
-    xn[(size_t)row * H_ + tid + 256] = y1;
-    xn_bf[(size_t)row * H_ + tid]       = f2bf(y0);
-    xn_bf[(size_t)row * H_ + tid + 256] = f2bf(y1);
-}
-
-__global__ void ew0_precompute(const float* __restrict__ bond_emb,
-                               const bf16* __restrict__ ewt0, bf16* __restrict__ E0) {
-    int t = blockIdx.x, cb = blockIdx.y, lane = threadIdx.x;
-    int c = cb * 64 + lane;
-    if (t >= 8) { E0[t * 512 + c] = f2bf(0.0f); return; }
-    __shared__ float be[512];
-    for (int h = lane; h < 512; h += 64) be[h] = bond_emb[t * 512 + h];
-    __syncthreads();
-    const bf16* wr = ewt0 + (size_t)c * 512;
-    float acc = 0.f;
-    for (int h8 = 0; h8 < 64; ++h8) {
-        uint4 u = *(const uint4*)(wr + h8 * 8);
-        float wf[8];
-        unpack8(u, wf);
-        const float* b = &be[h8 * 8];
-        acc += b[0]*wf[0] + b[1]*wf[1] + b[2]*wf[2] + b[3]*wf[3]
-             + b[4]*wf[4] + b[5]*wf[5] + b[6]*wf[6] + b[7]*wf[7];
-    }
-    E0[t * 512 + c] = f2bf(acc);
-}
-
-__global__ void transpose_sq(const float* __restrict__ Wq, const float* __restrict__ Wk,
-                             const float* __restrict__ Wv, const float* __restrict__ Wew,
-                             const float* __restrict__ Wst,
-                             bf16* __restrict__ qkvt, bf16* __restrict__ ewt,
-                             bf16* __restrict__ stackt) {
-    const size_t KN = (size_t)H_ * H_;
-    int z = blockIdx.z;
-    const float* W; bf16* Wt;
-    if (z < 12) {
-        int s = z >> 2, l = z & 3;
-        W  = (s == 0 ? Wq : s == 1 ? Wk : Wv) + (size_t)l * KN;
-        Wt = qkvt + (size_t)l * 3 * KN + (size_t)s * KN;
-    } else if (z < 16) {
-        int l = z - 12;
-        W = Wew + (size_t)l * KN; Wt = ewt + (size_t)l * KN;
-    } else {
-        int l = z - 16;
-        W = Wst + (size_t)l * KN; Wt = stackt + (size_t)l * KN;
-    }
-    __shared__ float t[32][33];
-    int k0 = blockIdx.x * 32, n0 = blockIdx.y * 32;
-    int tx = threadIdx.x, ty = threadIdx.y;
-    #pragma unroll
-    for (int r = ty; r < 32; r += 8)
-        t[r][tx] = W[(size_t)(k0 + r) * H_ + n0 + tx];
-    __syncthreads();
-    #pragma unroll
-    for (int r = ty; r < 32; r += 8)
-        Wt[(size_t)(n0 + r) * H_ + k0 + tx] = f2bf(t[tx][r]);
-}
-
-__global__ void transpose_rect(const float* __restrict__ Wf1, const float* __restrict__ Wf2,
-                               bf16* __restrict__ f1t, bf16* __restrict__ f2t) {
-    const size_t KN4 = (size_t)4 * H_ * H_;
-    int z = blockIdx.z;
-    const float* W; bf16* Wt; int K, N;
-    if (z < 4) {
-        if (blockIdx.x >= 16) return;
-        W = Wf1 + (size_t)z * KN4; Wt = f1t + (size_t)z * KN4; K = 512; N = 2048;
-    } else {
-        if (blockIdx.y >= 16) return;
-        W = Wf2 + (size_t)(z - 4) * KN4; Wt = f2t + (size_t)(z - 4) * KN4; K = 2048; N = 512;
-    }
-    __shared__ float t[32][33];
-    int k0 = blockIdx.x * 32, n0 = blockIdx.y * 32;
-    int tx = threadIdx.x, ty = threadIdx.y;
-    #pragma unroll
-    for (int r = ty; r < 32; r += 8)
-        t[r][tx] = W[(size_t)(k0 + r) * N + n0 + tx];
-    __syncthreads();
-    #pragma unroll
-    for (int r = ty; r < 32; r += 8)
-        Wt[(size_t)(n0 + r) * K + k0 + tx] = f2bf(t[tx][r]);
 }
 
 __global__ void reduce_stack_ln(const float* __restrict__ part, const float* __restrict__ base,
@@ -776,8 +866,13 @@
     o[(size_t)bi * H_ + h * 64 + d] = __float2bfloat16(oacc);
 }
 
-__global__ void attn3_kernel(const float* __restrict__ qkv, const float* __restrict__ s2,
-                             const int* __restrict__ adj, bf16* __restrict__ o) {
+__global__ void attn3s2_kernel(const float* __restrict__ qkv, const int* __restrict__ adj,
+        const float* __restrict__ c0a, const float* __restrict__ c1a, const float* __restrict__ c2a,
+        const float* __restrict__ c0b, const float* __restrict__ c1b, const float* __restrict__ c2b,
+        const float* __restrict__ v0c, const float* __restrict__ v1c, const float* __restrict__ v2c,
+        const float* __restrict__ MX, const float* __restrict__ MY,
+        const float* __restrict__ MZ, const float* __restrict__ DE,
+        bf16* __restrict__ o) {
     const float* q = qkv;
     const float* k = qkv + (size_t)512 * H_;
     const float* v = qkv + (size_t)1024 * H_;
@@ -791,26 +886,37 @@
     __syncthreads();
 
     int j = lane;
+    int p = bi * 64 + j;
+    int t = adj[p];
+    float v0 = v0c[p];
+    float q0 = v0 * c0b[p];
+    float AE = q0 * c0a[p], Aa = q0 * c1a[p], Ab = q0 * c2a[p];
+    float Ac = v0 * c1b[p], Ad = v0 * c2b[p];
+    float Ae = v1c[p], Af = v2c[p];
+    size_t rb = ((size_t)b * 512 + i * 8 + h) * 64;
+    float acc = AE * DE[rb + t]
+              + Aa * MX[rb + i] + Ac * MY[rb + i] + Ae * MZ[rb + i]
+              + Ab * MX[rb + j] + Ad * MY[rb + j] + Af * MZ[rb + j];
+
     const float4* k4 = (const float4*)(k + (size_t)(b * 64 + j) * H_ + h * 64);
-    float acc = s2[(((size_t)b * 8 + h) * 64 + i) * 64 + j];
-    #pragma unroll
-    for (int t = 0; t < 8; ++t) {
-        float4 ka = k4[2 * t], kb = k4[2 * t + 1];
-        const float* qq = &qs[ty][t * 8];
+    #pragma unroll
+    for (int tt = 0; tt < 8; ++tt) {
+        float4 ka = k4[2 * tt], kb = k4[2 * tt + 1];
+        const float* qq = &qs[ty][tt * 8];
         acc += qq[0] * ka.x + qq[1] * ka.y + qq[2] * ka.z + qq[3] * ka.w
              + qq[4] * kb.x + qq[5] * kb.y + qq[6] * kb.z + qq[7] * kb.w;
     }
     float logit = acc * INV_SCALE;
-    if (adj[(size_t)bi * 64 + j] <= 0) logit = -INFINITY;
+    if (t <= 0) logit = -INFINITY;
 
     float m = logit;
     #pragma unroll
     for (int off = 32; off; off >>= 1) m = fmaxf(m, __shfl_xor(m, off));
-    float p = expf(logit - m);
-    float s = p;
+    float pe = expf(logit - m);
+    float s = pe;
     #pragma unroll
     for (int off = 32; off; off >>= 1) s += __shfl_xor(s, off);
-    as[ty][lane] = p / s;
+    as[ty][lane] = pe / s;
     __syncthreads();
 
     const float* vbase = v + (size_t)(b * 64) * H_ + h * 64;
@@ -820,51 +926,6 @@
     for (int jj = 0; jj < 64; ++jj)
         oacc += as[ty][jj] * vbase[(size_t)jj * H_ + d];
     o[(size_t)bi * H_ + h * 64 + d] = __float2bfloat16(oacc);
-}
-
-template <bool GATHER>
-__global__ void edge_coeff_kernel(const bf16* __restrict__ ewsrc, const int* __restrict__ adj,
-                                  const float* __restrict__ x,
-                                  float* __restrict__ w0o, float* __restrict__ w1o,
-                                  float* __restrict__ w2o) {
-    int pair = blockIdx.x * 4 + threadIdx.y;
-    int b = pair >> 12;
-    int i = (pair >> 6) & 63;
-    int j = pair & 63;
-    int lane = threadIdx.x;
-    const uint4*  e4  = (const uint4*)(GATHER ? ewsrc + (size_t)adj[pair] * H_
-                                              : ewsrc + (size_t)pair * H_);
-    const float4* xi4 = (const float4*)(x + (size_t)(b * 64 + i) * H_);
-    const float4* xj4 = (const float4*)(x + (size_t)(b * 64 + j) * H_);
-    uint4  eu = e4[lane];
-    float4 a0 = xi4[lane * 2], a1 = xi4[lane * 2 + 1];
-    float4 c0 = xj4[lane * 2], c1 = xj4[lane * 2 + 1];
-    float ef[8], af[8], cf[8];
-    unpack8(eu, ef);
-    af[0] = a0.x; af[1] = a0.y; af[2] = a0.z; af[3] = a0.w;
-    af[4] = a1.x; af[5] = a1.y; af[6] = a1.z; af[7] = a1.w;
-    cf[0] = c0.x; cf[1] = c0.y; cf[2] = c0.z; cf[3] = c0.w;
-    cf[4] = c1.x; cf[5] = c1.y; cf[6] = c1.z; cf[7] = c1.w;
-    float s0 = 0.f, s1 = 0.f, s2 = 0.f;
-    #pragma unroll
-    for (int t = 0; t < 8; ++t) {
-        s0 += ef[t] * ef[t]; s1 += ef[t] * af[t]; s2 += ef[t] * cf[t];
-    }
-    #pragma unroll
-    for (int off = 32; off; off >>= 1) {
-        s0 += __shfl_xor(s0, off);
-        s1 += __shfl_xor(s1, off);
-        s2 += __shfl_xor(s2, off);
-    }
-    float t0 = s0 * INV_SCALE, t1 = s1 * INV_SCALE, t2 = s2 * INV_SCALE;
-    float m = fmaxf(t0, fmaxf(t1, t2));
-    float e0 = expf(t0 - m), e1 = expf(t1 - m), e2 = expf(t2 - m);
-    float inv = 1.0f / (e0 + e1 + e2);
-    if (lane == 0) {
-        w0o[pair] = e0 * inv;
-        w1o[pair] = e1 * inv;
-        w2o[pair] = e2 * inv;
-    }
 }
 
 __global__ void cls_part_kernel(const float* __restrict__ x, const float* __restrict__ Wout,
@@ -969,7 +1030,6 @@
     float* part    = (float*)(ws + alloc(4 * ROWS * H_ * 4));
     float* clspart = (float*)(ws + alloc(4 * 8 * H_ * 4));
     bf16*  ubf     = (bf16*) (ws + alloc(ROWS * 8 * 512 * 2));
-    float* s2buf   = (float*)(ws + alloc((size_t)B_ * 8 * 64 * 64 * 4));
     float* MX      = (float*)(ws + alloc((size_t)4096 * 64 * 4));
     float* MY      = (float*)(ws + alloc((size_t)4096 * 64 * 4));
     float* MZ      = (float*)(ws + alloc((size_t)4096 * 64 * 4));
@@ -1003,15 +1063,10 @@
     float* cw1c = cw + 7 * PAIRS;
     float* cw2c = cw + 8 * PAIRS;
 
-    embed_ln_kernel<<<512, 256, 0, stream>>>(ids, atom_emb, xn, xn_bf);
-
-    dim3 tb(32, 8);
-    transpose_sq<<<dim3(16, 16, 20), tb, 0, stream>>>(Wq, Wk, Wv, Wew, Wstack,
-                                                      qkvt, ewt, stackt);
-    transpose_rect<<<dim3(64, 64, 8), tb, 0, stream>>>(Wf1, Wf2, f1t, f2t);
-
-    ew0_precompute<<<dim3(64, 8), 64, 0, stream>>>(bond_emb, ewt, E0);
-    cast_w3<<<128, 256, 0, stream>>>(Wew + 3 * KN, wc3);
+    setup_kernel<<<14080, 256, 0, stream>>>(ids, atom_emb, bond_emb,
+                                            Wq, Wk, Wv, Wew, Wstack, Wf1, Wf2,
+                                            xn, xn_bf, qkvt, ewt, stackt, f1t, f2t,
+                                            E0, wc3);
 
     for (int l = 0; l < L_; ++l) {
         if (l == 0) {
@@ -1019,32 +1074,34 @@
                 xn_bf, qkvt, qkv, nullptr, 512, 512, 512);
             attn_kernel<true><<<dim3(512, 2), dim3(64, 4), 0, stream>>>(qkv, E0, adj, o_bf);
         } else if (l == 1) {
-            basis1_qkv_kernel<<<dim3(33, 8), 256, 0, stream>>>(
-                x_bf, E0, ewt + KN, xw1, e0w1, xn_bf, qkvt + (size_t)3 * KN, qkv);
-            ptable_kernel<<<dim3(8, 8, 2), 256, 0, stream>>>(
-                qkv, xw1, e0w1, nullptr, PT0, PT1, nullptr);
+            basis1_qkv_ec<<<2312, 256, 0, stream>>>(
+                x_bf, E0, ewt + KN, xw1, e0w1, xn_bf, qkvt + (size_t)3 * KN, qkv,
+                adj, x, cw0a, cw1a, cw2a);
+            ptable_kernel<<<dim3(8, 8, 2), 256, 0, stream>>>(qkv, xw1, e0w1, PT0, PT1);
             attn13_kernel<1><<<dim3(512, 2), dim3(64, 4), 0, stream>>>(
                 qkv, adj, cw0a, cw1a, cw2a, nullptr, nullptr, nullptr,
                 PT0, nullptr, PT1, o_bf);
         } else if (l == 2) {
-            basis2_qkv_kernel<<<dim3(41, 8), 256, 0, stream>>>(
+            basis2_qkv_g1<<<368, 256, 0, stream>>>(
                 xw1, x_bf, e0w1, ewt + 2 * KN, xw12, x2w2, e0w12,
-                xn_bf, qkvt + (size_t)6 * KN, qkv);
-            ptable_kernel<<<dim3(8, 8, 3), 256, 0, stream>>>(
-                qkv, xw12, x2w2, e0w12, PT0, PT1, PT2);
+                xn_bf, qkvt + (size_t)6 * KN, qkv, gbuf);
+            ptable2c<<<256, 256, 0, stream>>>(
+                qkv, xw12, x2w2, e0w12, PT0, PT1, PT2,
+                adj, cw0a, cw1a, cw2a, gbuf, cw0b, cw1b, cw2b);
             attn13_kernel<2><<<dim3(512, 2), dim3(64, 4), 0, stream>>>(
                 qkv, adj, cw0a, cw1a, cw2a, cw0b, cw1b, cw2b,
                 PT0, PT1, PT2, o_bf);
         } else {
-            mfma_gemm_s<0, false><<<dim3(8, 8, 3), 256, 0, stream>>>(
-                xn_bf, qkvt + (size_t)9 * KN, qkv, nullptr, 512, 512, 512);
-            u_gemm<<<dim3(8, 8, 8), 256, 0, stream>>>(qkv, wc3, ubf);
+            l3qkv_g2<<<264, 256, 0, stream>>>(
+                xn_bf, qkvt + (size_t)9 * KN, qkv, xw12, x2w2, e0w12, x_bf, gbuf);
+            u_c2<<<576, 256, 0, stream>>>(
+                qkv, wc3, ubf, adj, cw0a, cw1a, cw2a, cw0b, cw1b, cw2b,
+                gbuf, cw0c, cw1c, cw2c);
             mbuf_gemm<<<dim3(8, 8, 4), 256, 0, stream>>>(ubf, xw12, x2w2, x_bf, e0w12,
                                                          MX, MY, MZ, DE);
-            s2_assemble<<<512, dim3(64, 8), 0, stream>>>(adj,
-                cw0a, cw1a, cw2a, cw0b, cw1b, cw2b, cw0c, cw1c, cw2c,
-                MX, MY, MZ, DE, s2buf);
-            attn3_kernel<<<dim3(512, 2), dim3(64, 4), 0, stream>>>(qkv, s2buf, adj, o_bf);
+            attn3s2_kernel<<<dim3(512, 2), dim3(64, 4), 0, stream>>>(
+                qkv, adj, cw0a, cw1a, cw2a, cw0b, cw1b, cw2b, cw0c, cw1c, cw2c,
+                MX, MY, MZ, DE, o_bf);
         }
 
         mfma_gemm_s<0, true><<<dim3(8, 8, 4), 256, 0, stream>>>(
@@ -1058,20 +1115,6 @@
             reduce_ln_kernel<true><<<512, 256, 0, stream>>>(part, resid, x, x_bf, xn, xn_bf);
         else
             reduce_ln_kernel<false><<<512, 256, 0, stream>>>(part, resid, x, x_bf, xn, xn_bf);
-
-        if (l == 0) {
-            edge_coeff_kernel<true><<<8192, dim3(64, 4), 0, stream>>>(
-                E0, adj, x, cw0a, cw1a, cw2a);
-        } else if (l == 1) {
-            gram1_kernel<<<dim3(8, 5), 256, 0, stream>>>(xw1, e0w1, x_bf, gbuf);
-            coeff_assemble1<<<512, 64, 0, stream>>>(adj, cw0a, cw1a, cw2a, gbuf,
-                                                    cw0b, cw1b, cw2b);
-        } else if (l == 2) {
-            gram2_kernel<<<dim3(8, 9), 256, 0, stream>>>(xw12, x2w2, e0w12, x_bf, gbuf);
-            coeff_assemble2<<<512, 64, 0, stream>>>(adj, cw0a, cw1a, cw2a,
-                                                    cw0b, cw1b, cw2b, gbuf,
-                                                    cw0c, cw1c, cw2c);
-        }
     }
 
     cls_part_kernel<<<dim3(8, 8, 4), 256, 0, stream>>>(x, Wout, clspart);
```

Measured after the change: 382.4 us. 1.03x faster.
